# Kernel tuning notes

Hardware: AMD Instinct MI355X
Metric: run time of the kernel (lower is better)

The kernel has to match this reference:

```python
import jax, jax.numpy as jnp
import numpy as np

# fbank band edges (hp.bandmode == 'fbank'), 32 bands over 257 freq bins
EBAND = [0,3,5,8,10,13,15,18,22,25,29,33,38,42,48,53,59,66,73,80,89,97,107,117,128,140,153,167,183,199,216,256]

def _inverse_filter():
    f = np.zeros((len(EBAND), EBAND[-1] + 1), np.float32)
    for i in range(len(EBAND) - 1):
        w = EBAND[i + 1] - EBAND[i]
        for j in range(w):
            f[i, EBAND[i] + j] = 1.0 - j / w
            f[i + 1, EBAND[i] + j] = j / w
    return jnp.asarray(f)  # [32, 257]

def _glin(x, w):
    # GroupedLinear (DeepFilterNet-style, no bias): w [g, in/g, out/g]
    g, gi, go = w.shape
    y = jnp.einsum('...gi,gio->...go', x.reshape(x.shape[:-1] + (g, gi)), w)
    return y.reshape(x.shape[:-1] + (g * go,))

def _prelu(x, a):
    return jnp.where(x >= 0, x, a * x)

def _gru(x, wih, whh, bih, bhh):
    # single-layer torch-style GRU; x [T,B,I], wih/whh [3H, I/H]
    H = whh.shape[-1]
    h0 = jnp.zeros((x.shape[1], H), x.dtype)
    def step(h, xt):
        gi = xt @ wih.T + bih
        gh = h @ whh.T + bhh
        ir, iz, inn = jnp.split(gi, 3, axis=-1)
        hr, hz, hn = jnp.split(gh, 3, axis=-1)
        r = jax.nn.sigmoid(ir + hr)
        z = jax.nn.sigmoid(iz + hz)
        n = jnp.tanh(inn + r * hn)
        hnew = (1.0 - z) * n + z * h
        return hnew, hnew
    _, ys = jax.lax.scan(step, h0, x)
    return ys  # [T,B,H]

def _ggru_layer(x, wih, whh, bih, bhh):
    # grouped GRU layer: weights stacked on leading group axis
    g = wih.shape[0]
    T, B, I = x.shape
    xg = x.reshape(T, B, g, I // g).transpose(2, 0, 1, 3)  # [g,T,B,I/g]
    ys = jax.vmap(_gru)(xg, wih, whh, bih, bhh)            # [g,T,B,H/g]
    return ys.transpose(1, 2, 0, 3).reshape(T, B, -1)

def _shuffle(x, g):
    # channel shuffle between grouped GRU layers
    T, B, H = x.shape
    return x.reshape(T, B, -1, g).swapaxes(2, 3).reshape(T, B, H)

def _forward(main_input, spec, log_power_input, s1_fc_in_w, s1_fc_in_b,
             s1_gru_wih0, s1_gru_whh0, s1_gru_bih0, s1_gru_bhh0,
             s1_gru_wih1, s1_gru_whh1, s1_gru_bih1, s1_gru_bhh1,
             s1_fcout_w, fc_in_low_w, prelu_low, fc_in_high_w, prelu_high,
             gru_low_wih, gru_low_whh, gru_low_bih, gru_low_bhh,
             gru_high_wih, gru_high_whh, gru_high_bih, gru_high_bhh,
             fc_out_low_w, fc_out_high_w, ne, fc):
    B, _, T, F = main_input.shape
    # --- Stage1: pad time, unfold window, keep first ne+1 taps ---
    xp = jnp.pad(main_input, ((0, 0), (0, 0), (ne, ne), (0, 0)))
    win = jnp.stack([xp[:, :, k:k + T] for k in range(ne + 1)], axis=-1)  # [B,1,T,F,ne+1]
    x = win.reshape(B, T, F * (ne + 1))                                   # [B,T,64]
    x0 = (x @ s1_fc_in_w.T + s1_fc_in_b).transpose(1, 0, 2)               # [T,B,32]
    y1 = _gru(x0, s1_gru_wih0, s1_gru_whh0, s1_gru_bih0, s1_gru_bhh0)
    y2 = _gru(y1, s1_gru_wih1, s1_gru_whh1, s1_gru_bih1, s1_gru_bhh1)
    x1 = (y1 + y2).transpose(1, 0, 2)                                     # add_outputs; [B,T,32]
    band_mask = jax.nn.sigmoid(_glin(x1, s1_fcout_w))                     # [B,T,32]
    full_mask = (band_mask @ _inverse_filter()).transpose(0, 2, 1)        # [B,257,T]
    out = spec * full_mask[..., None]                                     # [B,257,T,2]
    # --- low band path ---
    low = jnp.concatenate([log_power_input[:, :, :fc], band_mask], axis=-1)  # [B,T,160]
    low = _prelu(_glin(low, fc_in_low_w), prelu_low).transpose(1, 0, 2)      # [T,B,64]
    acc = jnp.zeros_like(low)
    inp = low
    for l in range(2):  # 2 grouped layers, shuffle between, add_outputs
        inp = _ggru_layer(inp, gru_low_wih[l], gru_low_whh[l], gru_low_bih[l], gru_low_bhh[l])
        if l == 0:
            inp = _shuffle(inp, 2)
        acc = acc + inp
    mask_low = jax.nn.sigmoid(_glin(acc.transpose(1, 0, 2), fc_out_low_w))   # [B,T,128]
    # --- high band path ---
    high = jnp.concatenate([log_power_input[:, :, fc:256], band_mask], axis=-1)  # [B,T,160]
    high = _prelu(_glin(high, fc_in_high_w), prelu_high).transpose(1, 0, 2)      # [T,B,32]
    dfh = _ggru_layer(high, gru_high_wih, gru_high_whh, gru_high_bih, gru_high_bhh)
    mask_high = jax.nn.sigmoid(_glin(dfh.transpose(1, 0, 2), fc_out_high_w))     # [B,T,128]
    # --- fuse masks (rows: 0:fc low, fc:256 high, 256 passthrough) ---
    mask = jnp.concatenate([
        mask_low.transpose(0, 2, 1) * full_mask[:, :fc],
        mask_high.transpose(0, 2, 1) * full_mask[:, fc:256],
        full_mask[:, 256:257],
    ], axis=1)                                                            # [B,257,T]
    spec_out = mask[..., None] * out
    spec_mag = jnp.sqrt(spec_out[..., 0] ** 2 + spec_out[..., 1] ** 2)
    return full_mask, mask, spec_mag, spec_out

def setup_inputs():
    ks = iter(jax.random.split(jax.random.key(0), 48))
    rn = lambda shape, s=1.0: jax.random.normal(next(ks), shape, jnp.float32) * s
    B, T = 256, 256
    return {
        'main_input': rn((B, 1, T, 32)),
        'spec': rn((B, 257, T, 2)),
        'log_power_input': rn((B, T, 256)),
        'n_expand_fbank': 1,
        'freq_cut': 128,
        's1_fc_in_w': rn((32, 64), 0.125),
        's1_fc_in_b': rn((32,), 0.05),
        's1_gru_wih0': rn((96, 32), 0.18),
        's1_gru_whh0': rn((96, 32), 0.18),
        's1_gru_bih0': rn((96,), 0.05),
        's1_gru_bhh0': rn((96,), 0.05),
        's1_gru_wih1': rn((96, 32), 0.18),
        's1_gru_whh1': rn((96, 32), 0.18),
        's1_gru_bih1': rn((96,), 0.05),
        's1_gru_bhh1': rn((96,), 0.05),
        's1_fcout_w': rn((1, 32, 32), 0.18),
        'fc_in_low_w': rn((1, 160, 64), 0.08),
        'prelu_low': jnp.full((1,), 0.25, jnp.float32),
        'fc_in_high_w': rn((2, 80, 16), 0.11),
        'prelu_high': jnp.full((1,), 0.25, jnp.float32),
        'gru_low_wih': rn((2, 2, 96, 32), 0.18),
        'gru_low_whh': rn((2, 2, 96, 32), 0.18),
        'gru_low_bih': rn((2, 2, 96), 0.05),
        'gru_low_bhh': rn((2, 2, 96), 0.05),
        'gru_high_wih': rn((2, 48, 16), 0.25),
        'gru_high_whh': rn((2, 48, 16), 0.25),
        'gru_high_bih': rn((2, 48), 0.05),
        'gru_high_bhh': rn((2, 48), 0.05),
        'fc_out_low_w': rn((1, 64, 128), 0.125),
        'fc_out_high_w': rn((2, 16, 64), 0.25),
    }

def reference(main_input, spec, log_power_input, n_expand_fbank, freq_cut,
              s1_fc_in_w, s1_fc_in_b,
              s1_gru_wih0, s1_gru_whh0, s1_gru_bih0, s1_gru_bhh0,
              s1_gru_wih1, s1_gru_whh1, s1_gru_bih1, s1_gru_bhh1,
              s1_fcout_w, fc_in_low_w, prelu_low, fc_in_high_w, prelu_high,
              gru_low_wih, gru_low_whh, gru_low_bih, gru_low_bhh,
              gru_high_wih, gru_high_whh, gru_high_bih, gru_high_bhh,
              fc_out_low_w, fc_out_high_w):
    return _forward(main_input, spec, log_power_input, s1_fc_in_w, s1_fc_in_b,
                    s1_gru_wih0, s1_gru_whh0, s1_gru_bih0, s1_gru_bhh0,
                    s1_gru_wih1, s1_gru_whh1, s1_gru_bih1, s1_gru_bhh1,
                    s1_fcout_w, fc_in_low_w, prelu_low, fc_in_high_w, prelu_high,
                    gru_low_wih, gru_low_whh, gru_low_bih, gru_low_bhh,
                    gru_high_wih, gru_high_whh, gru_high_bih, gru_high_bhh,
                    fc_out_low_w, fc_out_high_w, int(n_expand_fbank), int(freq_cut))
```

## Files before the change

### kernel.cpp

```cpp
#include <hip/hip_runtime.h>
#include <math.h>

#define Bn 256
#define Tn 256

__constant__ int EB[32] = {0,3,5,8,10,13,15,18,22,25,29,33,38,42,48,53,59,66,73,80,89,97,107,117,128,140,153,167,183,199,216,256};

__device__ __forceinline__ float fsig(float x){ return __builtin_amdgcn_rcpf(1.f + __expf(-x)); }
__device__ __forceinline__ float ftanh(float x){ return 1.f - 2.f*__builtin_amdgcn_rcpf(1.f + __expf(2.f*x)); }

__device__ __forceinline__ void gload16(const float* g, float* l){
  __builtin_amdgcn_global_load_lds((const __attribute__((address_space(1))) void*)g,
                                   (__attribute__((address_space(3))) void*)l, 16, 0, 0);
}

#define KEEP(x) asm volatile("" : "+v"(x))

typedef float v2f __attribute__((ext_vector_type(2)));

#define DOT16(res, X, W) do{ float _s0=0.f,_s1=0.f,_s2=0.f,_s3=0.f; \
  _Pragma("unroll") for (int _e=0;_e<4;++_e){ \
    _s0=fmaf((X)[_e],(W)[_e],_s0); _s1=fmaf((X)[4+_e],(W)[4+_e],_s1); \
    _s2=fmaf((X)[8+_e],(W)[8+_e],_s2); _s3=fmaf((X)[12+_e],(W)[12+_e],_s3);} \
  (res)=(_s0+_s1)+(_s2+_s3); }while(0)

#define DOT8(res, X, W) do{ float _s0=0.f,_s1=0.f; \
  _Pragma("unroll") for (int _e=0;_e<4;++_e){ \
    _s0=fmaf((X)[_e],(W)[_e],_s0); _s1=fmaf((X)[4+_e],(W)[4+_e],_s1);} \
  (res)=_s0+_s1; }while(0)

#define FMA44(A, X, W) do{ \
  (A)[0]=fmaf((X).x,(W)[0].x,(A)[0]); (A)[1]=fmaf((X).x,(W)[0].y,(A)[1]); (A)[2]=fmaf((X).x,(W)[0].z,(A)[2]); (A)[3]=fmaf((X).x,(W)[0].w,(A)[3]); \
  (A)[0]=fmaf((X).y,(W)[1].x,(A)[0]); (A)[1]=fmaf((X).y,(W)[1].y,(A)[1]); (A)[2]=fmaf((X).y,(W)[1].z,(A)[2]); (A)[3]=fmaf((X).y,(W)[1].w,(A)[3]); \
  (A)[0]=fmaf((X).z,(W)[2].x,(A)[0]); (A)[1]=fmaf((X).z,(W)[2].y,(A)[1]); (A)[2]=fmaf((X).z,(W)[2].z,(A)[2]); (A)[3]=fmaf((X).z,(W)[2].w,(A)[3]); \
  (A)[0]=fmaf((X).w,(W)[3].x,(A)[0]); (A)[1]=fmaf((X).w,(W)[3].y,(A)[1]); (A)[2]=fmaf((X).w,(W)[3].z,(A)[2]); (A)[3]=fmaf((X).w,(W)[3].w,(A)[3]); \
}while(0)

__global__ __launch_bounds__(256) void k0(const float* __restrict__ wfc, const float* __restrict__ bfc,
    const float* __restrict__ wih0, const float* __restrict__ bih0,
    const float* __restrict__ wih1,
    const float* __restrict__ glw_ih, const float* __restrict__ glb_ih,
    const float* __restrict__ ghw_ih, const float* __restrict__ ghb_ih,
    float* __restrict__ wcT, float* __restrict__ bc,
    float* __restrict__ wBT, float* __restrict__ bB,
    float* __restrict__ wih1T, float* __restrict__ wB2T, float* __restrict__ bB2){
  int i = blockIdx.x*256 + threadIdx.x;
  if (i < 6144){
    int k = i/96, o = i - (i/96)*96;
    float s = 0.f;
    #pragma unroll
    for (int kk = 0; kk < 32; ++kk) s = fmaf(wih0[o*32+kk], wfc[kk*64+k], s);
    wcT[i] = s;
  } else if (i < 6240){
    int o = i - 6144;
    float s = bih0[o];
    #pragma unroll
    for (int kk = 0; kk < 32; ++kk) s = fmaf(wih0[o*32+kk], bfc[kk], s);
    bc[o] = s;
  } else if (i < 13920){
    int j = i - 6240;
    if (j < 6144){
      int og = j >> 7, rem = j & 127, k = rem >> 2, jj = rem & 3;
      int o = og*4 + jj; int g = o/96, r = o - g*96;
      wBT[j] = glw_ih[(g*96 + r)*32 + k];
    } else {
      int j2 = j - 6144;
      int oh = j2 >> 6, rem = j2 & 63, k = rem >> 2, jj = rem & 3;
      int o = oh*4 + jj; int g = o/48, r = o - g*48;
      wBT[j] = ghw_ih[(g*48 + r)*16 + k];
    }
  } else if (i < 14208){
    int o = i - 13920;
    bB[o] = (o < 192) ? glb_ih[o] : ghb_ih[o - 192];
  } else if (i < 17280){
    int j = i - 14208;
    int k = j/96, o = j - (j/96)*96;
    wih1T[j] = wih1[o*32 + k];
  } else if (i < 23424){
    int j = i - 17280;
    int og = j >> 7, rem = j & 127, k = rem >> 2, jj = rem & 3;
    int o = og*4 + jj; int g = o/96, r = o - g*96;
    wB2T[j] = glw_ih[((2+g)*96 + r)*32 + k];
  } else if (i < 23616){
    int o = i - 23424;
    bB2[o] = glb_ih[192 + o];
  }
}

__global__ __launch_bounds__(256) void k1(const float* __restrict__ mi,
    const float* __restrict__ wcT, const float* __restrict__ bc,
    float* __restrict__ gi0){
  __shared__ float mbuf[33*36];
  const int tid = threadIdx.x;
  const int b = blockIdx.x >> 3;
  const int t0 = (blockIdx.x & 7)*32;
  const int bt0 = b*256 + t0;
  for (int idx = tid; idx < 264; idx += 256){
    int row = idx >> 3, c4 = idx & 7;
    int r = t0 - 1 + row;
    float4 v = make_float4(0.f,0.f,0.f,0.f);
    if (r >= 0) v = *(const float4*)&mi[(b*256 + r)*32 + c4*4];
    *(float4*)&mbuf[row*36 + c4*4] = v;
  }
  __syncthreads();
  const int og = tid >> 3, btg = tid & 7;
  if (og >= 24) return;
  float acc[4][4];
  #pragma unroll
  for (int bj = 0; bj < 4; ++bj){ acc[bj][0]=0.f; acc[bj][1]=0.f; acc[bj][2]=0.f; acc[bj][3]=0.f; }
  for (int fq = 0; fq < 8; ++fq){
    float4 wvp[4], wvc[4];
    #pragma unroll
    for (int i = 0; i < 4; ++i){
      int f = fq*4 + i;
      wvp[i] = *(const float4*)&wcT[(2*f)*96 + og*4];
      wvc[i] = *(const float4*)&wcT[(2*f+1)*96 + og*4];
    }
    #pragma unroll
    for (int bj = 0; bj < 4; ++bj){
      int btl = btg + 8*bj;
      float4 xp = *(const float4*)&mbuf[btl*36 + fq*4];
      float4 xc = *(const float4*)&mbuf[(btl+1)*36 + fq*4];
      FMA44(acc[bj], xp, wvp);
      FMA44(acc[bj], xc, wvc);
    }
  }
  float4 bias = *(const float4*)&bc[og*4];
  #pragma unroll
  for (int bj = 0; bj < 4; ++bj){
    int btl = btg + 8*bj;
    float4 o;
    o.x = acc[bj][0] + bias.x; o.y = acc[bj][1] + bias.y;
    o.z = acc[bj][2] + bias.z; o.w = acc[bj][3] + bias.w;
    *(float4*)&gi0[(bt0 + btl)*96 + og*4] = o;
  }
}

__global__ __launch_bounds__(128,1) void kS1(const float* __restrict__ gi0,
    const float* __restrict__ whh0, const float* __restrict__ bhh0,
    const float* __restrict__ wih1, const float* __restrict__ whh1,
    const float* __restrict__ bih1, const float* __restrict__ bhh1,
    const float* __restrict__ fco, float* __restrict__ bmA)
{
  __shared__ __attribute__((aligned(16))) float gib[2][3072];
  __shared__ __attribute__((aligned(16))) float y1buf[2][32];
  __shared__ __attribute__((aligned(16))) float h1arr[32];
  __shared__ __attribute__((aligned(16))) float h2arr[32];
  const int tid = threadIdx.x;
  const int wid = tid >> 6;
  const int lane = tid & 63;
  const int q = lane >> 5, h = lane & 31, ko = q*16;
  const int b = blockIdx.x;
  const float* gsrc = gi0 + b*24576;

  float wI[3][16], wH[3][16], wF[16];
  float b0, b1, b2, b3;
  if (wid == 0){
    #pragma unroll
    for (int g = 0; g < 3; ++g){
      const float* w = whh0 + (g*32+h)*32 + ko;
      #pragma unroll
      for (int k = 0; k < 16; ++k){ wI[g][k] = w[k]; wH[g][k] = w[k]; }
    }
    #pragma unroll
    for (int k = 0; k < 16; ++k) wF[k] = 0.f;
    b0 = bhh0[h]; b1 = bhh0[32+h]; b2 = bhh0[64+h]; b3 = 0.f;
    #pragma unroll
    for (int c0 = 0; c0 < 2; ++c0)
      for (int it = 0; it < 12; ++it)
        gload16(gsrc + c0*3072 + it*256 + lane*4, &gib[c0][it*256]);
    asm volatile("s_waitcnt vmcnt(0)" ::: "memory");
  } else {
    #pragma unroll
    for (int g = 0; g < 3; ++g){
      const float* wi = wih1 + (g*32+h)*32 + ko;
      const float* wh = whh1 + (g*32+h)*32 + ko;
      #pragma unroll
      for (int k = 0; k < 16; ++k){ wI[g][k] = wi[k]; wH[g][k] = wh[k]; }
    }
    #pragma unroll
    for (int k = 0; k < 16; ++k) wF[k] = fco[(ko+k)*32 + h];
    b0 = bih1[h] + bhh1[h];
    b1 = bih1[32+h] + bhh1[32+h];
    b2 = bih1[64+h];
    b3 = bhh1[64+h];
  }
  #pragma unroll
  for (int g = 0; g < 3; ++g){
    #pragma unroll
    for (int k = 0; k < 16; ++k){ KEEP(wI[g][k]); KEEP(wH[g][k]); }
  }
  #pragma unroll
  for (int k = 0; k < 16; ++k) KEEP(wF[k]);
  __syncthreads();

  float hv[16];
  #pragma unroll
  for (int k = 0; k < 16; ++k) hv[k] = 0.f;
  float hOwn = 0.f;
  float c_r = 0.f, c_z = 0.f, c_n = 0.f, p_r = 0.f, p_z = 0.f, p_n = 0.f;

  for (int s = 0; s <= Tn; ++s){
    __syncthreads();
    if (wid == 0){
      if (s < Tn){
        const int t = s;
        if ((t & 31) == 0){
          if (t){
            int c = t >> 5;
            if (c < 7){
              for (int it = 0; it < 12; ++it)
                gload16(gsrc + (c+1)*3072 + it*256 + lane*4, &gib[(c+1)&1][it*256]);
            }
          }
          const float* gt = &gib[(t>>5)&1][(t&31)*96];
          c_r = gt[h]; c_z = gt[32+h]; c_n = gt[64+h];
        } else { c_r = p_r; c_z = p_z; c_n = p_n; }
        if ((t+1) & 31){
          const float* gn = &gib[((t+1)>>5)&1][((t+1)&31)*96];
          p_r = gn[h]; p_z = gn[32+h]; p_n = gn[64+h];
        }
        float pr, pz, pn;
        DOT16(pr, hv, wI[0]); DOT16(pz, hv, wI[1]); DOT16(pn, hv, wI[2]);
        pr += __shfl_xor(pr,32); pz += __shfl_xor(pz,32); pn += __shfl_xor(pn,32);
        float r = fsig(c_r + pr + b0);
        float z = fsig(c_z + pz + b1);
        float nn = ftanh(c_n + r*(pn + b2));
        float hn = nn + z*(hOwn - nn);
        hOwn = hn;
        h1arr[h] = hn;
        if (q == 0) y1buf[s & 1][h] = hn;
        *(float4*)&hv[0]  = *(const float4*)&h1arr[ko+0];
        *(float4*)&hv[4]  = *(const float4*)&h1arr[ko+4];
        *(float4*)&hv[8]  = *(const float4*)&h1arr[ko+8];
        *(float4*)&hv[12] = *(const float4*)&h1arr[ko+12];
      }
    } else {
      if (s >= 1){
        const int t = s - 1;
        const float* yb = y1buf[t & 1];
        float xv[16];
        *(float4*)&xv[0]  = *(const float4*)&yb[ko+0];
        *(float4*)&xv[4]  = *(const float4*)&yb[ko+4];
        *(float4*)&xv[8]  = *(const float4*)&yb[ko+8];
        *(float4*)&xv[12] = *(const float4*)&yb[ko+12];
        float ur, uz, ui, vr, vz, vh;
        DOT16(ur, xv, wI[0]); DOT16(uz, xv, wI[1]); DOT16(ui, xv, wI[2]);
        DOT16(vr, hv, wH[0]); DOT16(vz, hv, wH[1]); DOT16(vh, hv, wH[2]);
        float qr = ur + vr, qz = uz + vz;
        qr += __shfl_xor(qr,32); qz += __shfl_xor(qz,32);
        ui += __shfl_xor(ui,32); vh += __shfl_xor(vh,32);
        float r1 = fsig(qr + b0);
        float z1 = fsig(qz + b1);
        float n1 = ftanh(ui + b2 + r1*(vh + b3));
        float hn = n1 + z1*(hOwn - n1);
        hOwn = hn;
        h2arr[h] = hn;
        *(float4*)&hv[0]  = *(const float4*)&h2arr[ko+0];
        *(float4*)&hv[4]  = *(const float4*)&h2arr[ko+4];
        *(float4*)&hv[8]  = *(const float4*)&h2arr[ko+8];
        *(float4*)&hv[12] = *(const float4*)&h2arr[ko+12];
        float sf = 0.f;
        #pragma unroll
        for (int k = 0; k < 16; ++k) sf = fmaf(xv[k] + hv[k], wF[k], sf);
        sf += __shfl_xor(sf,32);
        if (q == 0) bmA[(b*Tn + t)*32 + h] = fsig(sf);
      }
    }
  }
}

__global__ __launch_bounds__(256) void kP(const float* __restrict__ lpi,
    const float* __restrict__ bmA,
    const float* __restrict__ wlo, const float* __restrict__ plo,
    const float* __restrict__ whi, const float* __restrict__ phi,
    const float* __restrict__ wBT, const float* __restrict__ bB,
    float* __restrict__ giL, float* __restrict__ giH)
{
  __shared__ float xb[32*292];
  __shared__ float mb[32*100];
  const int tid = threadIdx.x;
  const int b = blockIdx.x >> 3;
  const int t0 = (blockIdx.x & 7)*32;
  const int bt0 = b*256 + t0;
  #pragma unroll
  for (int j = 0; j < 8; ++j){
    int idx = j*256 + tid;
    int row = idx >> 6, c4 = idx & 63;
    float4 v = *(const float4*)&lpi[(bt0 + row)*256 + c4*4];
    *(float4*)&xb[row*292 + c4*4] = v;
  }
  {
    int row = tid >> 3, c4 = tid & 7;
    float4 v = *(const float4*)&bmA[(bt0 + row)*32 + c4*4];
    *(float4*)&xb[row*292 + 256 + c4*4] = v;
  }
  __syncthreads();
  const int og = tid >> 3, btg = tid & 7;
  if (og < 16){
    float acc[4][4];
    #pragma unroll
    for (int bj = 0; bj < 4; ++bj){ acc[bj][0]=0.f; acc[bj][1]=0.f; acc[bj][2]=0.f; acc[bj][3]=0.f; }
    for (int kq = 0; kq < 40; ++kq){
      int k0_ = kq*4;
      int kk = (k0_ < 128) ? k0_ : k0_ + 128;
      float4 wv[4];
      #pragma unroll
      for (int i = 0; i < 4; ++i) wv[i] = *(const float4*)&wlo[(k0_+i)*64 + og*4];
      #pragma unroll
      for (int bj = 0; bj < 4; ++bj){
        float4 xv = *(const float4*)&xb[(btg + 8*bj)*292 + kk];
        FMA44(acc[bj], xv, wv);
      }
    }
    const float a = plo[0];
    #pragma unroll
    for (int bj = 0; bj < 4; ++bj){
      float4 m;
      m.x = acc[bj][0] >= 0.f ? acc[bj][0] : a*acc[bj][0];
      m.y = acc[bj][1] >= 0.f ? acc[bj][1] : a*acc[bj][1];
      m.z = acc[bj][2] >= 0.f ? acc[bj][2] : a*acc[bj][2];
      m.w = acc[bj][3] >= 0.f ? acc[bj][3] : a*acc[bj][3];
      *(float4*)&mb[(btg + 8*bj)*100 + og*4] = m;
    }
  } else if (og < 24){
    int o0 = (og - 16)*4;
    int g = o0 >> 4, r0 = o0 & 15;
    int xoff = 128 + g*80;
    float acc[4][4];
    #pragma unroll
    for (int bj = 0; bj < 4; ++bj){ acc[bj][0]=0.f; acc[bj][1]=0.f; acc[bj][2]=0.f; acc[bj][3]=0.f; }
    for (int kq = 0; kq < 20; ++kq){
      int k0_ = kq*4;
      float4 wv[4];
      #pragma unroll
      for (int i = 0; i < 4; ++i) wv[i] = *(const float4*)&whi[(g*80 + k0_ + i)*16 + r0];
      #pragma unroll
      for (int bj = 0; bj < 4; ++bj){
        float4 xv = *(const float4*)&xb[(btg + 8*bj)*292 + xoff + k0_];
        FMA44(acc[bj], xv, wv);
      }
    }
    const float a = phi[0];
    #pragma unroll
    for (int bj = 0; bj < 4; ++bj){
      float4 m;
      m.x = acc[bj][0] >= 0.f ? acc[bj][0] : a*acc[bj][0];
      m.y = acc[bj][1] >= 0.f ? acc[bj][1] : a*acc[bj][1];
      m.z = acc[bj][2] >= 0.f ? acc[bj][2] : a*acc[bj][2];
      m.w = acc[bj][3] >= 0.f ? acc[bj][3] : a*acc[bj][3];
      *(float4*)&mb[(btg + 8*bj)*100 + 64 + o0] = m;
    }
  }
  __syncthreads();
  for (int og2 = og; og2 < 72; og2 += 32){
    int woff, kbase, K, obase, dstride;
    float* dst;
    float4 bias;
    if (og2 < 48){
      woff = og2*128; kbase = (og2 >= 24) ? 32 : 0; K = 32;
      obase = og2*4; dst = giL; dstride = 192;
      bias = *(const float4*)&bB[obase];
    } else {
      int oh = og2 - 48;
      woff = 6144 + oh*64;
      int o0 = oh*4; int g = o0/48;
      kbase = 64 + g*16; K = 16;
      obase = o0; dst = giH; dstride = 96;
      bias = *(const float4*)&bB[192 + o0];
    }
    float acc[4][4];
    #pragma unroll
    for (int bj = 0; bj < 4; ++bj){ acc[bj][0]=0.f; acc[bj][1]=0.f; acc[bj][2]=0.f; acc[bj][3]=0.f; }
    for (int kq = 0; kq < K/4; ++kq){
      float4 wv[4];
      #pragma unroll
      for (int i = 0; i < 4; ++i) wv[i] = *(const float4*)&wBT[woff + (kq*4 + i)*4];
      #pragma unroll
      for (int bj = 0; bj < 4; ++bj){
        float4 xv = *(const float4*)&mb[(btg + 8*bj)*100 + kbase + kq*4];
        FMA44(acc[bj], xv, wv);
      }
    }
    #pragma unroll
    for (int bj = 0; bj < 4; ++bj){
      int btl = btg + 8*bj;
      float4 o;
      o.x = acc[bj][0] + bias.x; o.y = acc[bj][1] + bias.y;
      o.z = acc[bj][2] + bias.z; o.w = acc[bj][3] + bias.w;
      *(float4*)&dst[(bt0 + btl)*dstride + obase] = o;
    }
  }
}

__global__ __launch_bounds__(256,1) void kR2(const float* __restrict__ giL,
    const float* __restrict__ giH,
    const float* __restrict__ wihL, const float* __restrict__ whhL,
    const float* __restrict__ bihL, const float* __restrict__ bhhL,
    const float* __restrict__ whhH, const float* __restrict__ bhhH,
    float* __restrict__ acc, float* __restrict__ dfh)
{
  __shared__ __attribute__((aligned(16))) float smem[12544];
  const int tid = threadIdx.x;
  const int wid = tid >> 6;
  const int lane = tid & 63;
  if (blockIdx.x < 256){
    const int role = wid >> 1;
    const int g = wid & 1;
    const int q = lane >> 5, h = lane & 31, ko = q*16;
    const int b = blockIdx.x;
    float* gib   = smem + g*6144;
    float* y0buf = smem + 12288;
    float* h0arr = smem + 12416 + g*32;
    float* h1l   = smem + 12480;
    const float* gsrc = giL + b*49152 + g*96;

    float wI[3][16], wH[3][16];
    float b0, b1, b2, b3;
    if (role == 0){
      #pragma unroll
      for (int gt = 0; gt < 3; ++gt){
        const float* w = whhL + (g*96 + gt*32 + h)*32 + ko;
        #pragma unroll
        for (int k = 0; k < 16; ++k){ wI[gt][k] = w[k]; wH[gt][k] = w[k]; }
      }
      b0 = bhhL[g*96+h]; b1 = bhhL[g*96+32+h]; b2 = bhhL[g*96+64+h]; b3 = 0.f;
      #pragma unroll
      for (int c0 = 0; c0 < 2; ++c0)
        for (int it = 0; it < 12; ++it){
          int i = it*64 + lane;
          int toff = i/24, c4 = i - toff*24;
          gload16(gsrc + (c0*32 + toff)*192 + c4*4, &gib[c0*3072 + it*256]);
        }
      asm volatile("s_waitcnt vmcnt(0)" ::: "memory");
    } else {
      #pragma unroll
      for (int gt = 0; gt < 3; ++gt){
        const float* wi = wihL + ((2+g)*96 + gt*32 + h)*32 + ko;
        const float* wh = whhL + ((2+g)*96 + gt*32 + h)*32 + ko;
        #pragma unroll
        for (int k = 0; k < 16; ++k){ wI[gt][k] = wi[k]; wH[gt][k] = wh[k]; }
      }
      b0 = bihL[(2+g)*96+h]    + bhhL[(2+g)*96+h];
      b1 = bihL[(2+g)*96+32+h] + bhhL[(2+g)*96+32+h];
      b2 = bihL[(2+g)*96+64+h];
      b3 = bhhL[(2+g)*96+64+h];
    }
    #pragma unroll
    for (int gt = 0; gt < 3; ++gt){
      #pragma unroll
      for (int k = 0; k < 16; ++k){ KEEP(wI[gt][k]); KEEP(wH[gt][k]); }
    }
    __syncthreads();

    float hv[16];
    #pragma unroll
    for (int k = 0; k < 16; ++k) hv[k] = 0.f;
    float hOwn = 0.f;
    float c_r = 0.f, c_z = 0.f, c_n = 0.f, p_r = 0.f, p_z = 0.f, p_n = 0.f;
    const int spos = ((h&1)<<5) + (g<<4) + (h>>1);

    for (int s = 0; s <= Tn; ++s){
      __syncthreads();
      if (role == 0){
        if (s < Tn){
          const int t = s;
          if ((t & 31) == 0){
            if (t){
              int c = t >> 5;
              if (c < 7){
                for (int it = 0; it < 12; ++it){
                  int i = it*64 + lane;
                  int toff = i/24, c4 = i - toff*24;
                  gload16(gsrc + ((c+1)*32 + toff)*192 + c4*4, &gib[((c+1)&1)*3072 + it*256]);
                }
              }
            }
            const float* gt = &gib[((t>>5)&1)*3072 + (t&31)*96];
            c_r = gt[h]; c_z = gt[32+h]; c_n = gt[64+h];
          } else { c_r = p_r; c_z = p_z; c_n = p_n; }
          if ((t+1) & 31){
            const float* gn = &gib[(((t+1)>>5)&1)*3072 + ((t+1)&31)*96];
            p_r = gn[h]; p_z = gn[32+h]; p_n = gn[64+h];
          }
          float pr, pz, pn;
          DOT16(pr, hv, wI[0]); DOT16(pz, hv, wI[1]); DOT16(pn, hv, wI[2]);
          pr += __shfl_xor(pr,32); pz += __shfl_xor(pz,32); pn += __shfl_xor(pn,32);
          float r = fsig(c_r + pr + b0);
          float z = fsig(c_z + pz + b1);
          float nn = ftanh(c_n + r*(pn + b2));
          float hn = nn + z*(hOwn - nn);
          hOwn = hn;
          h0arr[h] = hn;
          if (q == 0) y0buf[(s&1)*64 + spos] = hn;
          *(float4*)&hv[0]  = *(const float4*)&h0arr[ko+0];
          *(float4*)&hv[4]  = *(const float4*)&h0arr[ko+4];
          *(float4*)&hv[8]  = *(const float4*)&h0arr[ko+8];
          *(float4*)&hv[12] = *(const float4*)&h0arr[ko+12];
        }
      } else {
        if (s >= 1){
          const int t = s - 1;
          const float* yb = &y0buf[(t&1)*64];
          float xv[16];
          *(float4*)&xv[0]  = *(const float4*)&yb[g*32 + ko + 0];
          *(float4*)&xv[4]  = *(const float4*)&yb[g*32 + ko + 4];
          *(float4*)&xv[8]  = *(const float4*)&yb[g*32 + ko + 8];
          *(float4*)&xv[12] = *(const float4*)&yb[g*32 + ko + 12];
          float yown = yb[g*32 + h];
          float ur, uz, ui, vr, vz, vh;
          DOT16(ur, xv, wI[0]); DOT16(uz, xv, wI[1]); DOT16(ui, xv, wI[2]);
          DOT16(vr, hv, wH[0]); DOT16(vz, hv, wH[1]); DOT16(vh, hv, wH[2]);
          float qr = ur + vr, qz = uz + vz;
          qr += __shfl_xor(qr,32); qz += __shfl_xor(qz,32);
          ui += __shfl_xor(ui,32); vh += __shfl_xor(vh,32);
          float r1 = fsig(qr + b0);
          float z1 = fsig(qz + b1);
          float n1 = ftanh(ui + b2 + r1*(vh + b3));
          float hn = n1 + z1*(hOwn - n1);
          hOwn = hn;
          h1l[g*32 + h] = hn;
          *(float4*)&hv[0]  = *(const float4*)&h1l[g*32 + ko+0];
          *(float4*)&hv[4]  = *(const float4*)&h1l[g*32 + ko+4];
          *(float4*)&hv[8]  = *(const float4*)&h1l[g*32 + ko+8];
          *(float4*)&hv[12] = *(const float4*)&h1l[g*32 + ko+12];
          if (q == 0) acc[(b*256 + t)*64 + g*32 + h] = yown + hn;
        }
      }
    }
  } else {
    const int g = lane >> 5, qh = (lane >> 4) & 1, h = lane & 15, ko = qh*8;
    const int b = (blockIdx.x - 256)*4 + wid;
    float* gib  = smem + wid*3072;
    float* harr = smem + 12288 + wid*32;
    float ah[3][8];
    #pragma unroll
    for (int gt = 0; gt < 3; ++gt){
      const float* wp = whhH + (g*48 + gt*16 + h)*16 + ko;
      #pragma unroll
      for (int k = 0; k < 8; ++k) ah[gt][k] = wp[k];
    }
    #pragma unroll
    for (int gt = 0; gt < 3; ++gt){
      #pragma unroll
      for (int k = 0; k < 8; ++k) KEEP(ah[gt][k]);
    }
    const float bhr = bhhH[g*48+h], bhz = bhhH[g*48+16+h], bhn = bhhH[g*48+32+h];
    const float* gsrc = giH + b*24576;
    #pragma unroll
    for (int c0 = 0; c0 < 2; ++c0)
      for (int it = 0; it < 6; ++it)
        gload16(gsrc + c0*1536 + it*256 + lane*4, &gib[c0*1536 + it*256]);
    asm volatile("s_waitcnt vmcnt(0)" ::: "memory");

    float hv[8];
    #pragma unroll
    for (int k = 0; k < 8; ++k) hv[k] = 0.f;
    float hOwn = 0.f;
    float c_r = 0.f, c_z = 0.f, c_n = 0.f, p_r = 0.f, p_z = 0.f, p_n = 0.f;

    for (int t = 0; t < Tn; ++t){
      if ((t & 15) == 0){
        if (t){
          int c = t >> 4;
          if (c < 15){
            const float* gs = gsrc + (c+1)*1536;
            for (int it = 0; it < 6; ++it)
              gload16(gs + it*256 + lane*4, &gib[((c+1)&1)*1536 + it*256]);
            asm volatile("s_waitcnt vmcnt(6)" ::: "memory");
          } else {
            asm volatile("s_waitcnt vmcnt(0)" ::: "memory");
          }
        }
        const float* gt = &gib[((t>>4)&1)*1536 + (t&15)*96 + g*48];
        c_r = gt[h]; c_z = gt[16+h]; c_n = gt[32+h];
      } else { c_r = p_r; c_z = p_z; c_n = p_n; }
      if ((t+1) & 15){
        const float* gn = &gib[(((t+1)>>4)&1)*1536 + ((t+1)&15)*96 + g*48];
        p_r = gn[h]; p_z = gn[16+h]; p_n = gn[32+h];
      }
      float pr, pz, pn;
      DOT8(pr, hv, ah[0]); DOT8(pz, hv, ah[1]); DOT8(pn, hv, ah[2]);
      pr += __shfl_xor(pr,16); pz += __shfl_xor(pz,16); pn += __shfl_xor(pn,16);
      float r = fsig(c_r + pr + bhr);
      float z = fsig(c_z + pz + bhz);
      float nn = ftanh(c_n + r*(pn + bhn));
      float hn = nn + z*(hOwn - nn);
      hOwn = hn;
      harr[g*16 + h] = hn;
      *(float4*)&hv[0] = *(const float4*)&harr[g*16 + ko + 0];
      *(float4*)&hv[4] = *(const float4*)&harr[g*16 + ko + 4];
      if (qh == 0) dfh[(b*256 + t)*32 + g*16 + h] = hn;
    }
  }
}

__global__ __launch_bounds__(256) void k7(const float* __restrict__ acc,
    const float* __restrict__ dfh, const float* __restrict__ bmA,
    const float* __restrict__ wlo, const float* __restrict__ whi,
    const float* __restrict__ spec, float* __restrict__ out)
{
  __shared__ float accs[32][65];
  __shared__ float dfhs[32][33];
  __shared__ float bmt[32][33];
  __shared__ float frcs[257];
  __shared__ int   ibds[257];
  const int tid = threadIdx.x;
  const int b  = blockIdx.x >> 3;
  const int t0 = (blockIdx.x & 7) * 32;
  for (int idx = tid; idx < 32*16; idx += 256){
    int tl = idx >> 4, c4 = (idx & 15)*4;
    float4 v = *(const float4*)&acc[(b*256 + t0 + tl)*64 + c4];
    accs[tl][c4] = v.x; accs[tl][c4+1] = v.y; accs[tl][c4+2] = v.z; accs[tl][c4+3] = v.w;
  }
  for (int idx = tid; idx < 32*8; idx += 256){
    int tl = idx >> 3, c4 = (idx & 7)*4;
    float4 v = *(const float4*)&dfh[(b*256 + t0 + tl)*32 + c4];
    dfhs[tl][c4] = v.x; dfhs[tl][c4+1] = v.y; dfhs[tl][c4+2] = v.z; dfhs[tl][c4+3] = v.w;
    float4 u = *(const float4*)&bmA[(b*Tn + t0 + tl)*32 + c4];
    bmt[tl][c4] = u.x; bmt[tl][c4+1] = u.y; bmt[tl][c4+2] = u.z; bmt[tl][c4+3] = u.w;
  }
  for (int f = tid; f < 257; f += 256){
    int i = 0;
    #pragma unroll
    for (int k = 1; k < 31; ++k) if (f >= EB[k]) i = k;
    ibds[f] = i;
    frcs[f] = (f < 256) ? (float)(f - EB[i]) / (float)(EB[i+1] - EB[i]) : 0.f;
  }
  __syncthreads();
  const int tl = tid & 31, fo = tid >> 5;
  float* out1 = out + 16842752;
  float* out2 = out + 2*16842752;
  float* out3 = out + 3*16842752;
  const float2* sp2 = (const float2*)spec;
  {
    float p[16];
    #pragma unroll
    for (int j = 0; j < 16; ++j) p[j] = 0.f;
    for (int i = 0; i < 64; ++i){
      float a = accs[tl][i];
      const float4* wr = (const float4*)&wlo[i*128 + fo*16];
      #pragma unroll
      for (int j4 = 0; j4 < 4; ++j4){
        float4 wv = wr[j4];
        p[j4*4+0] = fmaf(a, wv.x, p[j4*4+0]);
        p[j4*4+1] = fmaf(a, wv.y, p[j4*4+1]);
        p[j4*4+2] = fmaf(a, wv.z, p[j4*4+2]);
        p[j4*4+3] = fmaf(a, wv.w, p[j4*4+3]);
      }
    }
    #pragma unroll
    for (int j = 0; j < 16; ++j){
      int f = fo*16 + j;
      int i = ibds[f]; float fr = frcs[f];
      float full = bmt[tl][i]*(1.f - fr) + bmt[tl][i+1]*fr;
      float m = fsig(p[j])*full;
      int base = (b*257 + f)*Tn + t0 + tl;
      float2 s = sp2[base];
      float fm = full*m;
      float sx = s.x*fm, sy = s.y*fm;
      __builtin_nontemporal_store(full, &out[base]);
      __builtin_nontemporal_store(m, &out1[base]);
      __builtin_nontemporal_store(sqrtf(sx*sx + sy*sy), &out2[base]);
      v2f o3; o3.x = sx; o3.y = sy;
      __builtin_nontemporal_store(o3, (v2f*)&out3[base*2]);
    }
  }
  {
    float p[16];
    #pragma unroll
    for (int j = 0; j < 16; ++j) p[j] = 0.f;
    const int g = fo >> 2, ob = (fo & 3)*16;
    for (int i = 0; i < 16; ++i){
      float a = dfhs[tl][g*16 + i];
      const float4* wr = (const float4*)&whi[(g*16 + i)*64 + ob];
      #pragma unroll
      for (int j4 = 0; j4 < 4; ++j4){
        float4 wv = wr[j4];
        p[j4*4+0] = fmaf(a, wv.x, p[j4*4+0]);
        p[j4*4+1] = fmaf(a, wv.y, p[j4*4+1]);
        p[j4*4+2] = fmaf(a, wv.z, p[j4*4+2]);
        p[j4*4+3] = fmaf(a, wv.w, p[j4*4+3]);
      }
    }
    #pragma unroll
    for (int j = 0; j < 16; ++j){
      int f = 128 + fo*16 + j;
      int i = ibds[f]; float fr = frcs[f];
      float full = bmt[tl][i]*(1.f - fr) + bmt[tl][i+1]*fr;
      float m = fsig(p[j])*full;
      int base = (b*257 + f)*Tn + t0 + tl;
      float2 s = sp2[base];
      float fm = full*m;
      float sx = s.x*fm, sy = s.y*fm;
      __builtin_nontemporal_store(full, &out[base]);
      __builtin_nontemporal_store(m, &out1[base]);
      __builtin_nontemporal_store(sqrtf(sx*sx + sy*sy), &out2[base]);
      v2f o3; o3.x = sx; o3.y = sy;
      __builtin_nontemporal_store(o3, (v2f*)&out3[base*2]);
    }
  }
  if (fo == 0){
    int base = (b*257 + 256)*Tn + t0 + tl;
    __builtin_nontemporal_store(0.f, &out[base]);
    __builtin_nontemporal_store(0.f, &out1[base]);
    __builtin_nontemporal_store(0.f, &out2[base]);
    v2f z; z.x = 0.f; z.y = 0.f;
    __builtin_nontemporal_store(z, (v2f*)&out3[base*2]);
  }
}

extern "C" void kernel_launch(void* const* d_in, const int* in_sizes, int n_in,
                              void* d_out, int out_size, void* d_ws, size_t ws_size,
                              hipStream_t stream){
  const float* mi   = (const float*)d_in[0];
  const float* spec = (const float*)d_in[1];
  const float* lpi  = (const float*)d_in[2];
  const float* s1w  = (const float*)d_in[5];
  const float* s1b  = (const float*)d_in[6];
  const float* wih0 = (const float*)d_in[7];
  const float* whh0 = (const float*)d_in[8];
  const float* bih0 = (const float*)d_in[9];
  const float* bhh0 = (const float*)d_in[10];
  const float* wih1 = (const float*)d_in[11];
  const float* whh1 = (const float*)d_in[12];
  const float* bih1 = (const float*)d_in[13];
  const float* bhh1 = (const float*)d_in[14];
  const float* fco  = (const float*)d_in[15];
  const float* filw = (const float*)d_in[16];
  const float* plo  = (const float*)d_in[17];
  const float* fihw = (const float*)d_in[18];
  const float* phi  = (const float*)d_in[19];
  const float* glw_ih = (const float*)d_in[20];
  const float* glw_hh = (const float*)d_in[21];
  const float* glb_ih = (const float*)d_in[22];
  const float* glb_hh = (const float*)d_in[23];
  const float* ghw_ih = (const float*)d_in[24];
  const float* ghw_hh = (const float*)d_in[25];
  const float* ghb_ih = (const float*)d_in[26];
  const float* ghb_hh = (const float*)d_in[27];
  const float* folw = (const float*)d_in[28];
  const float* fohw = (const float*)d_in[29];

  float* outf = (float*)d_out;
  float* giL  = outf;
  float* gi0  = outf + 12582912;
  float* giH  = outf + 18874368;

  float* ws    = (float*)d_ws;
  float* wcT   = ws;
  float* bc    = ws + 6144;
  float* wBT   = ws + 6240;
  float* bB    = ws + 13920;
  float* wih1T = ws + 14208;
  float* wB2T  = ws + 17280;
  float* bB2   = ws + 23424;
  float* bmA   = ws + 24576;
  float* acc   = ws + 2121728;
  float* dfh   = ws + 6316032;
  float* out   = (float*)d_out;

  k0<<<93, 256, 0, stream>>>(s1w, s1b, wih0, bih0, wih1, glw_ih, glb_ih, ghw_ih, ghb_ih,
                             wcT, bc, wBT, bB, wih1T, wB2T, bB2);
  k1<<<2048, 256, 0, stream>>>(mi, wcT, bc, gi0);
  kS1<<<256, 128, 0, stream>>>(gi0, whh0, bhh0, wih1, whh1, bih1, bhh1, fco, bmA);
  kP<<<2048, 256, 0, stream>>>(lpi, bmA, filw, plo, fihw, phi, wBT, bB, giL, giH);
  kR2<<<320, 256, 0, stream>>>(giL, giH, glw_ih, glw_hh, glb_ih, glb_hh,
                               ghw_hh, ghb_hh, acc, dfh);
  k7<<<2048, 256, 0, stream>>>(acc, dfh, bmA, folw, fohw, spec, out);
}
```

Measured before the change: 578.4 us.

## Fuse projection, stage-1 GRU, pointwise and grouped GRU kernels into one per-batch kernel

Merges k1, kS1, kP and kR2 into a single kernel kM with one 320-thread block per batch element. Each block runs the input projection, the stage-1 GRU, the middle projections and the low/high grouped GRUs in sequence, and drops the unused transposed-weight outputs from k0. This removes several launches and the gaps between them, and keeps intermediates hot in cache. The cost is only 256 blocks doing the formerly 2048-block parallel projections, and one block per CU under heavy register pressure.

```diff
diff --git a/kernel.cpp b/kernel.cpp
--- a/kernel.cpp
+++ b/kernel.cpp
@@ -38,12 +38,10 @@
 
 __global__ __launch_bounds__(256) void k0(const float* __restrict__ wfc, const float* __restrict__ bfc,
     const float* __restrict__ wih0, const float* __restrict__ bih0,
-    const float* __restrict__ wih1,
     const float* __restrict__ glw_ih, const float* __restrict__ glb_ih,
     const float* __restrict__ ghw_ih, const float* __restrict__ ghb_ih,
     float* __restrict__ wcT, float* __restrict__ bc,
-    float* __restrict__ wBT, float* __restrict__ bB,
-    float* __restrict__ wih1T, float* __restrict__ wB2T, float* __restrict__ bB2){
+    float* __restrict__ wBT, float* __restrict__ bB){
   int i = blockIdx.x*256 + threadIdx.x;
   if (i < 6144){
     int k = i/96, o = i - (i/96)*96;
@@ -72,385 +70,132 @@
   } else if (i < 14208){
     int o = i - 13920;
     bB[o] = (o < 192) ? glb_ih[o] : ghb_ih[o - 192];
-  } else if (i < 17280){
-    int j = i - 14208;
-    int k = j/96, o = j - (j/96)*96;
-    wih1T[j] = wih1[o*32 + k];
-  } else if (i < 23424){
-    int j = i - 17280;
-    int og = j >> 7, rem = j & 127, k = rem >> 2, jj = rem & 3;
-    int o = og*4 + jj; int g = o/96, r = o - g*96;
-    wB2T[j] = glw_ih[((2+g)*96 + r)*32 + k];
-  } else if (i < 23616){
-    int o = i - 23424;
-    bB2[o] = glb_ih[192 + o];
   }
 }
 
-__global__ __launch_bounds__(256) void k1(const float* __restrict__ mi,
+__global__ __launch_bounds__(320,1) void kM(const float* __restrict__ mi,
     const float* __restrict__ wcT, const float* __restrict__ bc,
-    float* __restrict__ gi0){
-  __shared__ float mbuf[33*36];
-  const int tid = threadIdx.x;
-  const int b = blockIdx.x >> 3;
-  const int t0 = (blockIdx.x & 7)*32;
-  const int bt0 = b*256 + t0;
-  for (int idx = tid; idx < 264; idx += 256){
-    int row = idx >> 3, c4 = idx & 7;
-    int r = t0 - 1 + row;
-    float4 v = make_float4(0.f,0.f,0.f,0.f);
-    if (r >= 0) v = *(const float4*)&mi[(b*256 + r)*32 + c4*4];
-    *(float4*)&mbuf[row*36 + c4*4] = v;
-  }
-  __syncthreads();
-  const int og = tid >> 3, btg = tid & 7;
-  if (og >= 24) return;
-  float acc[4][4];
-  #pragma unroll
-  for (int bj = 0; bj < 4; ++bj){ acc[bj][0]=0.f; acc[bj][1]=0.f; acc[bj][2]=0.f; acc[bj][3]=0.f; }
-  for (int fq = 0; fq < 8; ++fq){
-    float4 wvp[4], wvc[4];
-    #pragma unroll
-    for (int i = 0; i < 4; ++i){
-      int f = fq*4 + i;
-      wvp[i] = *(const float4*)&wcT[(2*f)*96 + og*4];
-      wvc[i] = *(const float4*)&wcT[(2*f+1)*96 + og*4];
-    }
-    #pragma unroll
-    for (int bj = 0; bj < 4; ++bj){
-      int btl = btg + 8*bj;
-      float4 xp = *(const float4*)&mbuf[btl*36 + fq*4];
-      float4 xc = *(const float4*)&mbuf[(btl+1)*36 + fq*4];
-      FMA44(acc[bj], xp, wvp);
-      FMA44(acc[bj], xc, wvc);
-    }
-  }
-  float4 bias = *(const float4*)&bc[og*4];
-  #pragma unroll
-  for (int bj = 0; bj < 4; ++bj){
-    int btl = btg + 8*bj;
-    float4 o;
-    o.x = acc[bj][0] + bias.x; o.y = acc[bj][1] + bias.y;
-    o.z = acc[bj][2] + bias.z; o.w = acc[bj][3] + bias.w;
-    *(float4*)&gi0[(bt0 + btl)*96 + og*4] = o;
-  }
-}
-
-__global__ __launch_bounds__(128,1) void kS1(const float* __restrict__ gi0,
     const float* __restrict__ whh0, const float* __restrict__ bhh0,
     const float* __restrict__ wih1, const float* __restrict__ whh1,
     const float* __restrict__ bih1, const float* __restrict__ bhh1,
-    const float* __restrict__ fco, float* __restrict__ bmA)
+    const float* __restrict__ fco,
+    const float* __restrict__ lpi,
+    const float* __restrict__ wlo, const float* __restrict__ plo,
+    const float* __restrict__ whi, const float* __restrict__ phi,
+    const float* __restrict__ wBT, const float* __restrict__ bB,
+    const float* __restrict__ wihL, const float* __restrict__ whhL,
+    const float* __restrict__ bihL, const float* __restrict__ bhhL,
+    const float* __restrict__ whhH, const float* __restrict__ bhhH,
+    float* __restrict__ gi0w, float* __restrict__ bmA,
+    float* __restrict__ giL, float* __restrict__ giH,
+    float* __restrict__ acc, float* __restrict__ dfh)
 {
-  __shared__ __attribute__((aligned(16))) float gib[2][3072];
-  __shared__ __attribute__((aligned(16))) float y1buf[2][32];
-  __shared__ __attribute__((aligned(16))) float h1arr[32];
-  __shared__ __attribute__((aligned(16))) float h2arr[32];
+  __shared__ __attribute__((aligned(16))) float smem[15648];
   const int tid = threadIdx.x;
   const int wid = tid >> 6;
   const int lane = tid & 63;
-  const int q = lane >> 5, h = lane & 31, ko = q*16;
   const int b = blockIdx.x;
-  const float* gsrc = gi0 + b*24576;
-
-  float wI[3][16], wH[3][16], wF[16];
-  float b0, b1, b2, b3;
-  if (wid == 0){
+
+  {
+    float* mbuf = smem;
+    for (int tile = 0; tile < 8; ++tile){
+      const int t0 = tile*32;
+      const int bt0 = b*256 + t0;
+      for (int idx = tid; idx < 264; idx += 320){
+        int row = idx >> 3, c4 = idx & 7;
+        int r = t0 - 1 + row;
+        float4 v = make_float4(0.f,0.f,0.f,0.f);
+        if (r >= 0) v = *(const float4*)&mi[(b*256 + r)*32 + c4*4];
+        *(float4*)&mbuf[row*36 + c4*4] = v;
+      }
+      __syncthreads();
+      if (tid < 256){
+        const int og = tid >> 3, btg = tid & 7;
+        if (og < 24){
+          float a4[4][4];
+          #pragma unroll
+          for (int bj = 0; bj < 4; ++bj){ a4[bj][0]=0.f; a4[bj][1]=0.f; a4[bj][2]=0.f; a4[bj][3]=0.f; }
+          for (int fq = 0; fq < 8; ++fq){
+            float4 wvp[4], wvc[4];
+            #pragma unroll
+            for (int i = 0; i < 4; ++i){
+              int f = fq*4 + i;
+              wvp[i] = *(const float4*)&wcT[(2*f)*96 + og*4];
+              wvc[i] = *(const float4*)&wcT[(2*f+1)*96 + og*4];
+            }
+            #pragma unroll
+            for (int bj = 0; bj < 4; ++bj){
+              int btl = btg + 8*bj;
+              float4 xp = *(const float4*)&mbuf[btl*36 + fq*4];
+              float4 xc = *(const float4*)&mbuf[(btl+1)*36 + fq*4];
+              FMA44(a4[bj], xp, wvp);
+              FMA44(a4[bj], xc, wvc);
+            }
+          }
+          float4 bias = *(const float4*)&bc[og*4];
+          #pragma unroll
+          for (int bj = 0; bj < 4; ++bj){
+            int btl = btg + 8*bj;
+            float4 o;
+            o.x = a4[bj][0] + bias.x; o.y = a4[bj][1] + bias.y;
+            o.z = a4[bj][2] + bias.z; o.w = a4[bj][3] + bias.w;
+            *(float4*)&gi0w[(bt0 + btl)*96 + og*4] = o;
+          }
+        }
+      }
+      __syncthreads();
+    }
+  }
+
+  {
+    const int q = lane >> 5, h = lane & 31, ko = q*16;
+    float* y1buf = smem + 6144;
+    float* h1arr = smem + 6208;
+    float* h2arr = smem + 6240;
+    const float* gsrc = gi0w + b*24576;
+    float wI[3][16], wH[3][16], wF[16];
+    float b0=0.f, b1=0.f, b2=0.f, b3=0.f;
+    #pragma unroll
+    for (int g = 0; g < 3; ++g)
+      #pragma unroll
+      for (int k = 0; k < 16; ++k){ wI[g][k]=0.f; wH[g][k]=0.f; }
+    #pragma unroll
+    for (int k = 0; k < 16; ++k) wF[k] = 0.f;
+    if (wid == 0){
+      #pragma unroll
+      for (int g = 0; g < 3; ++g){
+        const float* w = whh0 + (g*32+h)*32 + ko;
+        #pragma unroll
+        for (int k = 0; k < 16; ++k){ wI[g][k] = w[k]; wH[g][k] = w[k]; }
+      }
+      b0 = bhh0[h]; b1 = bhh0[32+h]; b2 = bhh0[64+h];
+      #pragma unroll
+      for (int c0 = 0; c0 < 2; ++c0)
+        for (int it = 0; it < 12; ++it)
+          gload16(gsrc + c0*3072 + it*256 + lane*4, &smem[c0*3072 + it*256]);
+      asm volatile("s_waitcnt vmcnt(0)" ::: "memory");
+    } else if (wid == 1){
+      #pragma unroll
+      for (int g = 0; g < 3; ++g){
+        const float* wi = wih1 + (g*32+h)*32 + ko;
+        const float* wh = whh1 + (g*32+h)*32 + ko;
+        #pragma unroll
+        for (int k = 0; k < 16; ++k){ wI[g][k] = wi[k]; wH[g][k] = wh[k]; }
+      }
+      #pragma unroll
+      for (int k = 0; k < 16; ++k) wF[k] = fco[(ko+k)*32 + h];
+      b0 = bih1[h] + bhh1[h];
+      b1 = bih1[32+h] + bhh1[32+h];
+      b2 = bih1[64+h];
+      b3 = bhh1[64+h];
+    }
     #pragma unroll
     for (int g = 0; g < 3; ++g){
-      const float* w = whh0 + (g*32+h)*32 + ko;
-      #pragma unroll
-      for (int k = 0; k < 16; ++k){ wI[g][k] = w[k]; wH[g][k] = w[k]; }
-    }
-    #pragma unroll
-    for (int k = 0; k < 16; ++k) wF[k] = 0.f;
-    b0 = bhh0[h]; b1 = bhh0[32+h]; b2 = bhh0[64+h]; b3 = 0.f;
-    #pragma unroll
-    for (int c0 = 0; c0 < 2; ++c0)
-      for (int it = 0; it < 12; ++it)
-        gload16(gsrc + c0*3072 + it*256 + lane*4, &gib[c0][it*256]);
-    asm volatile("s_waitcnt vmcnt(0)" ::: "memory");
-  } else {
-    #pragma unroll
-    for (int g = 0; g < 3; ++g){
-      const float* wi = wih1 + (g*32+h)*32 + ko;
-      const float* wh = whh1 + (g*32+h)*32 + ko;
-      #pragma unroll
-      for (int k = 0; k < 16; ++k){ wI[g][k] = wi[k]; wH[g][k] = wh[k]; }
-    }
-    #pragma unroll
-    for (int k = 0; k < 16; ++k) wF[k] = fco[(ko+k)*32 + h];
-    b0 = bih1[h] + bhh1[h];
-    b1 = bih1[32+h] + bhh1[32+h];
-    b2 = bih1[64+h];
-    b3 = bhh1[64+h];
-  }
-  #pragma unroll
-  for (int g = 0; g < 3; ++g){
-    #pragma unroll
-    for (int k = 0; k < 16; ++k){ KEEP(wI[g][k]); KEEP(wH[g][k]); }
-  }
-  #pragma unroll
-  for (int k = 0; k < 16; ++k) KEEP(wF[k]);
-  __syncthreads();
-
-  float hv[16];
-  #pragma unroll
-  for (int k = 0; k < 16; ++k) hv[k] = 0.f;
-  float hOwn = 0.f;
-  float c_r = 0.f, c_z = 0.f, c_n = 0.f, p_r = 0.f, p_z = 0.f, p_n = 0.f;
-
-  for (int s = 0; s <= Tn; ++s){
-    __syncthreads();
-    if (wid == 0){
-      if (s < Tn){
-        const int t = s;
-        if ((t & 31) == 0){
-          if (t){
-            int c = t >> 5;
-            if (c < 7){
-              for (int it = 0; it < 12; ++it)
-                gload16(gsrc + (c+1)*3072 + it*256 + lane*4, &gib[(c+1)&1][it*256]);
-            }
-          }
-          const float* gt = &gib[(t>>5)&1][(t&31)*96];
-          c_r = gt[h]; c_z = gt[32+h]; c_n = gt[64+h];
-        } else { c_r = p_r; c_z = p_z; c_n = p_n; }
-        if ((t+1) & 31){
-          const float* gn = &gib[((t+1)>>5)&1][((t+1)&31)*96];
-          p_r = gn[h]; p_z = gn[32+h]; p_n = gn[64+h];
-        }
-        float pr, pz, pn;
-        DOT16(pr, hv, wI[0]); DOT16(pz, hv, wI[1]); DOT16(pn, hv, wI[2]);
-        pr += __shfl_xor(pr,32); pz += __shfl_xor(pz,32); pn += __shfl_xor(pn,32);
-        float r = fsig(c_r + pr + b0);
-        float z = fsig(c_z + pz + b1);
-        float nn = ftanh(c_n + r*(pn + b2));
-        float hn = nn + z*(hOwn - nn);
-        hOwn = hn;
-        h1arr[h] = hn;
-        if (q == 0) y1buf[s & 1][h] = hn;
-        *(float4*)&hv[0]  = *(const float4*)&h1arr[ko+0];
-        *(float4*)&hv[4]  = *(const float4*)&h1arr[ko+4];
-        *(float4*)&hv[8]  = *(const float4*)&h1arr[ko+8];
-        *(float4*)&hv[12] = *(const float4*)&h1arr[ko+12];
-      }
-    } else {
-      if (s >= 1){
-        const int t = s - 1;
-        const float* yb = y1buf[t & 1];
-        float xv[16];
-        *(float4*)&xv[0]  = *(const float4*)&yb[ko+0];
-        *(float4*)&xv[4]  = *(const float4*)&yb[ko+4];
-        *(float4*)&xv[8]  = *(const float4*)&yb[ko+8];
-        *(float4*)&xv[12] = *(const float4*)&yb[ko+12];
-        float ur, uz, ui, vr, vz, vh;
-        DOT16(ur, xv, wI[0]); DOT16(uz, xv, wI[1]); DOT16(ui, xv, wI[2]);
-        DOT16(vr, hv, wH[0]); DOT16(vz, hv, wH[1]); DOT16(vh, hv, wH[2]);
-        float qr = ur + vr, qz = uz + vz;
-        qr += __shfl_xor(qr,32); qz += __shfl_xor(qz,32);
-        ui += __shfl_xor(ui,32); vh += __shfl_xor(vh,32);
-        float r1 = fsig(qr + b0);
-        float z1 = fsig(qz + b1);
-        float n1 = ftanh(ui + b2 + r1*(vh + b3));
-        float hn = n1 + z1*(hOwn - n1);
-        hOwn = hn;
-        h2arr[h] = hn;
-        *(float4*)&hv[0]  = *(const float4*)&h2arr[ko+0];
-        *(float4*)&hv[4]  = *(const float4*)&h2arr[ko+4];
-        *(float4*)&hv[8]  = *(const float4*)&h2arr[ko+8];
-        *(float4*)&hv[12] = *(const float4*)&h2arr[ko+12];
-        float sf = 0.f;
-        #pragma unroll
-        for (int k = 0; k < 16; ++k) sf = fmaf(xv[k] + hv[k], wF[k], sf);
-        sf += __shfl_xor(sf,32);
-        if (q == 0) bmA[(b*Tn + t)*32 + h] = fsig(sf);
-      }
-    }
-  }
-}
-
-__global__ __launch_bounds__(256) void kP(const float* __restrict__ lpi,
-    const float* __restrict__ bmA,
-    const float* __restrict__ wlo, const float* __restrict__ plo,
-    const float* __restrict__ whi, const float* __restrict__ phi,
-    const float* __restrict__ wBT, const float* __restrict__ bB,
-    float* __restrict__ giL, float* __restrict__ giH)
-{
-  __shared__ float xb[32*292];
-  __shared__ float mb[32*100];
-  const int tid = threadIdx.x;
-  const int b = blockIdx.x >> 3;
-  const int t0 = (blockIdx.x & 7)*32;
-  const int bt0 = b*256 + t0;
-  #pragma unroll
-  for (int j = 0; j < 8; ++j){
-    int idx = j*256 + tid;
-    int row = idx >> 6, c4 = idx & 63;
-    float4 v = *(const float4*)&lpi[(bt0 + row)*256 + c4*4];
-    *(float4*)&xb[row*292 + c4*4] = v;
-  }
-  {
-    int row = tid >> 3, c4 = tid & 7;
-    float4 v = *(const float4*)&bmA[(bt0 + row)*32 + c4*4];
-    *(float4*)&xb[row*292 + 256 + c4*4] = v;
-  }
-  __syncthreads();
-  const int og = tid >> 3, btg = tid & 7;
-  if (og < 16){
-    float acc[4][4];
-    #pragma unroll
-    for (int bj = 0; bj < 4; ++bj){ acc[bj][0]=0.f; acc[bj][1]=0.f; acc[bj][2]=0.f; acc[bj][3]=0.f; }
-    for (int kq = 0; kq < 40; ++kq){
-      int k0_ = kq*4;
-      int kk = (k0_ < 128) ? k0_ : k0_ + 128;
-      float4 wv[4];
-      #pragma unroll
-      for (int i = 0; i < 4; ++i) wv[i] = *(const float4*)&wlo[(k0_+i)*64 + og*4];
-      #pragma unroll
-      for (int bj = 0; bj < 4; ++bj){
-        float4 xv = *(const float4*)&xb[(btg + 8*bj)*292 + kk];
-        FMA44(acc[bj], xv, wv);
-      }
-    }
-    const float a = plo[0];
-    #pragma unroll
-    for (int bj = 0; bj < 4; ++bj){
-      float4 m;
-      m.x = acc[bj][0] >= 0.f ? acc[bj][0] : a*acc[bj][0];
-      m.y = acc[bj][1] >= 0.f ? acc[bj][1] : a*acc[bj][1];
-      m.z = acc[bj][2] >= 0.f ? acc[bj][2] : a*acc[bj][2];
-      m.w = acc[bj][3] >= 0.f ? acc[bj][3] : a*acc[bj][3];
-      *(float4*)&mb[(btg + 8*bj)*100 + og*4] = m;
-    }
-  } else if (og < 24){
-    int o0 = (og - 16)*4;
-    int g = o0 >> 4, r0 = o0 & 15;
-    int xoff = 128 + g*80;
-    float acc[4][4];
-    #pragma unroll
-    for (int bj = 0; bj < 4; ++bj){ acc[bj][0]=0.f; acc[bj][1]=0.f; acc[bj][2]=0.f; acc[bj][3]=0.f; }
-    for (int kq = 0; kq < 20; ++kq){
-      int k0_ = kq*4;
-      float4 wv[4];
-      #pragma unroll
-      for (int i = 0; i < 4; ++i) wv[i] = *(const float4*)&whi[(g*80 + k0_ + i)*16 + r0];
-      #pragma unroll
-      for (int bj = 0; bj < 4; ++bj){
-        float4 xv = *(const float4*)&xb[(btg + 8*bj)*292 + xoff + k0_];
-        FMA44(acc[bj], xv, wv);
-      }
-    }
-    const float a = phi[0];
-    #pragma unroll
-    for (int bj = 0; bj < 4; ++bj){
-      float4 m;
-      m.x = acc[bj][0] >= 0.f ? acc[bj][0] : a*acc[bj][0];
-      m.y = acc[bj][1] >= 0.f ? acc[bj][1] : a*acc[bj][1];
-      m.z = acc[bj][2] >= 0.f ? acc[bj][2] : a*acc[bj][2];
-      m.w = acc[bj][3] >= 0.f ? acc[bj][3] : a*acc[bj][3];
-      *(float4*)&mb[(btg + 8*bj)*100 + 64 + o0] = m;
-    }
-  }
-  __syncthreads();
-  for (int og2 = og; og2 < 72; og2 += 32){
-    int woff, kbase, K, obase, dstride;
-    float* dst;
-    float4 bias;
-    if (og2 < 48){
-      woff = og2*128; kbase = (og2 >= 24) ? 32 : 0; K = 32;
-      obase = og2*4; dst = giL; dstride = 192;
-      bias = *(const float4*)&bB[obase];
-    } else {
-      int oh = og2 - 48;
-      woff = 6144 + oh*64;
-      int o0 = oh*4; int g = o0/48;
-      kbase = 64 + g*16; K = 16;
-      obase = o0; dst = giH; dstride = 96;
-      bias = *(const float4*)&bB[192 + o0];
-    }
-    float acc[4][4];
-    #pragma unroll
-    for (int bj = 0; bj < 4; ++bj){ acc[bj][0]=0.f; acc[bj][1]=0.f; acc[bj][2]=0.f; acc[bj][3]=0.f; }
-    for (int kq = 0; kq < K/4; ++kq){
-      float4 wv[4];
-      #pragma unroll
-      for (int i = 0; i < 4; ++i) wv[i] = *(const float4*)&wBT[woff + (kq*4 + i)*4];
-      #pragma unroll
-      for (int bj = 0; bj < 4; ++bj){
-        float4 xv = *(const float4*)&mb[(btg + 8*bj)*100 + kbase + kq*4];
-        FMA44(acc[bj], xv, wv);
-      }
-    }
-    #pragma unroll
-    for (int bj = 0; bj < 4; ++bj){
-      int btl = btg + 8*bj;
-      float4 o;
-      o.x = acc[bj][0] + bias.x; o.y = acc[bj][1] + bias.y;
-      o.z = acc[bj][2] + bias.z; o.w = acc[bj][3] + bias.w;
-      *(float4*)&dst[(bt0 + btl)*dstride + obase] = o;
-    }
-  }
-}
-
-__global__ __launch_bounds__(256,1) void kR2(const float* __restrict__ giL,
-    const float* __restrict__ giH,
-    const float* __restrict__ wihL, const float* __restrict__ whhL,
-    const float* __restrict__ bihL, const float* __restrict__ bhhL,
-    const float* __restrict__ whhH, const float* __restrict__ bhhH,
-    float* __restrict__ acc, float* __restrict__ dfh)
-{
-  __shared__ __attribute__((aligned(16))) float smem[12544];
-  const int tid = threadIdx.x;
-  const int wid = tid >> 6;
-  const int lane = tid & 63;
-  if (blockIdx.x < 256){
-    const int role = wid >> 1;
-    const int g = wid & 1;
-    const int q = lane >> 5, h = lane & 31, ko = q*16;
-    const int b = blockIdx.x;
-    float* gib   = smem + g*6144;
-    float* y0buf = smem + 12288;
-    float* h0arr = smem + 12416 + g*32;
-    float* h1l   = smem + 12480;
-    const float* gsrc = giL + b*49152 + g*96;
-
-    float wI[3][16], wH[3][16];
-    float b0, b1, b2, b3;
-    if (role == 0){
-      #pragma unroll
-      for (int gt = 0; gt < 3; ++gt){
-        const float* w = whhL + (g*96 + gt*32 + h)*32 + ko;
-        #pragma unroll
-        for (int k = 0; k < 16; ++k){ wI[gt][k] = w[k]; wH[gt][k] = w[k]; }
-      }
-      b0 = bhhL[g*96+h]; b1 = bhhL[g*96+32+h]; b2 = bhhL[g*96+64+h]; b3 = 0.f;
-      #pragma unroll
-      for (int c0 = 0; c0 < 2; ++c0)
-        for (int it = 0; it < 12; ++it){
-          int i = it*64 + lane;
-          int toff = i/24, c4 = i - toff*24;
-          gload16(gsrc + (c0*32 + toff)*192 + c4*4, &gib[c0*3072 + it*256]);
-        }
-      asm volatile("s_waitcnt vmcnt(0)" ::: "memory");
-    } else {
-      #pragma unroll
-      for (int gt = 0; gt < 3; ++gt){
-        const float* wi = wihL + ((2+g)*96 + gt*32 + h)*32 + ko;
-        const float* wh = whhL + ((2+g)*96 + gt*32 + h)*32 + ko;
-        #pragma unroll
-        for (int k = 0; k < 16; ++k){ wI[gt][k] = wi[k]; wH[gt][k] = wh[k]; }
-      }
-      b0 = bihL[(2+g)*96+h]    + bhhL[(2+g)*96+h];
-      b1 = bihL[(2+g)*96+32+h] + bhhL[(2+g)*96+32+h];
-      b2 = bihL[(2+g)*96+64+h];
-      b3 = bhhL[(2+g)*96+64+h];
-    }
-    #pragma unroll
-    for (int gt = 0; gt < 3; ++gt){
-      #pragma unroll
-      for (int k = 0; k < 16; ++k){ KEEP(wI[gt][k]); KEEP(wH[gt][k]); }
-    }
+      #pragma unroll
+      for (int k = 0; k < 16; ++k){ KEEP(wI[g][k]); KEEP(wH[g][k]); }
+    }
+    #pragma unroll
+    for (int k = 0; k < 16; ++k) KEEP(wF[k]);
     __syncthreads();
 
     float hv[16];
@@ -458,29 +203,25 @@
     for (int k = 0; k < 16; ++k) hv[k] = 0.f;
     float hOwn = 0.f;
     float c_r = 0.f, c_z = 0.f, c_n = 0.f, p_r = 0.f, p_z = 0.f, p_n = 0.f;
-    const int spos = ((h&1)<<5) + (g<<4) + (h>>1);
 
     for (int s = 0; s <= Tn; ++s){
       __syncthreads();
-      if (role == 0){
+      if (wid == 0){
         if (s < Tn){
           const int t = s;
           if ((t & 31) == 0){
             if (t){
               int c = t >> 5;
               if (c < 7){
-                for (int it = 0; it < 12; ++it){
-                  int i = it*64 + lane;
-                  int toff = i/24, c4 = i - toff*24;
-                  gload16(gsrc + ((c+1)*32 + toff)*192 + c4*4, &gib[((c+1)&1)*3072 + it*256]);
-                }
+                for (int it = 0; it < 12; ++it)
+                  gload16(gsrc + (c+1)*3072 + it*256 + lane*4, &smem[((c+1)&1)*3072 + it*256]);
               }
             }
-            const float* gt = &gib[((t>>5)&1)*3072 + (t&31)*96];
+            const float* gt = &smem[((t>>5)&1)*3072 + (t&31)*96];
             c_r = gt[h]; c_z = gt[32+h]; c_n = gt[64+h];
           } else { c_r = p_r; c_z = p_z; c_n = p_n; }
           if ((t+1) & 31){
-            const float* gn = &gib[(((t+1)>>5)&1)*3072 + ((t+1)&31)*96];
+            const float* gn = &smem[(((t+1)>>5)&1)*3072 + ((t+1)&31)*96];
             p_r = gn[h]; p_z = gn[32+h]; p_n = gn[64+h];
           }
           float pr, pz, pn;
@@ -491,23 +232,22 @@
           float nn = ftanh(c_n + r*(pn + b2));
           float hn = nn + z*(hOwn - nn);
           hOwn = hn;
-          h0arr[h] = hn;
-          if (q == 0) y0buf[(s&1)*64 + spos] = hn;
-          *(float4*)&hv[0]  = *(const float4*)&h0arr[ko+0];
-          *(float4*)&hv[4]  = *(const float4*)&h0arr[ko+4];
-          *(float4*)&hv[8]  = *(const float4*)&h0arr[ko+8];
-          *(float4*)&hv[12] = *(const float4*)&h0arr[ko+12];
-        }
-      } else {
+          h1arr[h] = hn;
+          if (q == 0) y1buf[(s & 1)*32 + h] = hn;
+          *(float4*)&hv[0]  = *(const float4*)&h1arr[ko+0];
+          *(float4*)&hv[4]  = *(const float4*)&h1arr[ko+4];
+          *(float4*)&hv[8]  = *(const float4*)&h1arr[ko+8];
+          *(float4*)&hv[12] = *(const float4*)&h1arr[ko+12];
+        }
+      } else if (wid == 1){
         if (s >= 1){
           const int t = s - 1;
-          const float* yb = &y0buf[(t&1)*64];
+          const float* yb = &y1buf[(t & 1)*32];
           float xv[16];
-          *(float4*)&xv[0]  = *(const float4*)&yb[g*32 + ko + 0];
-          *(float4*)&xv[4]  = *(const float4*)&yb[g*32 + ko + 4];
-          *(float4*)&xv[8]  = *(const float4*)&yb[g*32 + ko + 8];
-          *(float4*)&xv[12] = *(const float4*)&yb[g*32 + ko + 12];
-          float yown = yb[g*32 + h];
+          *(float4*)&xv[0]  = *(const float4*)&yb[ko+0];
+          *(float4*)&xv[4]  = *(const float4*)&yb[ko+4];
+          *(float4*)&xv[8]  = *(const float4*)&yb[ko+8];
+          *(float4*)&xv[12] = *(const float4*)&yb[ko+12];
           float ur, uz, ui, vr, vz, vh;
           DOT16(ur, xv, wI[0]); DOT16(uz, xv, wI[1]); DOT16(ui, xv, wI[2]);
           DOT16(vr, hv, wH[0]); DOT16(vz, hv, wH[1]); DOT16(vh, hv, wH[2]);
@@ -519,78 +259,328 @@
           float n1 = ftanh(ui + b2 + r1*(vh + b3));
           float hn = n1 + z1*(hOwn - n1);
           hOwn = hn;
-          h1l[g*32 + h] = hn;
-          *(float4*)&hv[0]  = *(const float4*)&h1l[g*32 + ko+0];
-          *(float4*)&hv[4]  = *(const float4*)&h1l[g*32 + ko+4];
-          *(float4*)&hv[8]  = *(const float4*)&h1l[g*32 + ko+8];
-          *(float4*)&hv[12] = *(const float4*)&h1l[g*32 + ko+12];
-          if (q == 0) acc[(b*256 + t)*64 + g*32 + h] = yown + hn;
-        }
-      }
-    }
-  } else {
-    const int g = lane >> 5, qh = (lane >> 4) & 1, h = lane & 15, ko = qh*8;
-    const int b = (blockIdx.x - 256)*4 + wid;
-    float* gib  = smem + wid*3072;
-    float* harr = smem + 12288 + wid*32;
-    float ah[3][8];
+          h2arr[h] = hn;
+          *(float4*)&hv[0]  = *(const float4*)&h2arr[ko+0];
+          *(float4*)&hv[4]  = *(const float4*)&h2arr[ko+4];
+          *(float4*)&hv[8]  = *(const float4*)&h2arr[ko+8];
+          *(float4*)&hv[12] = *(const float4*)&h2arr[ko+12];
+          float sf = 0.f;
+          #pragma unroll
+          for (int k = 0; k < 16; ++k) sf = fmaf(xv[k] + hv[k], wF[k], sf);
+          sf += __shfl_xor(sf,32);
+          if (q == 0) bmA[(b*Tn + t)*32 + h] = fsig(sf);
+        }
+      }
+    }
+    __syncthreads();
+  }
+
+  {
+    float* xb = smem;
+    float* mb = smem + 9344;
+    for (int tile = 0; tile < 8; ++tile){
+      const int t0 = tile*32;
+      const int bt0 = b*256 + t0;
+      if (tid < 256){
+        #pragma unroll
+        for (int j = 0; j < 8; ++j){
+          int idx = j*256 + tid;
+          int row = idx >> 6, c4 = idx & 63;
+          float4 v = *(const float4*)&lpi[(bt0 + row)*256 + c4*4];
+          *(float4*)&xb[row*292 + c4*4] = v;
+        }
+        {
+          int row = tid >> 3, c4 = tid & 7;
+          float4 v = *(const float4*)&bmA[(bt0 + row)*32 + c4*4];
+          *(float4*)&xb[row*292 + 256 + c4*4] = v;
+        }
+      }
+      __syncthreads();
+      if (tid < 256){
+        const int og = tid >> 3, btg = tid & 7;
+        if (og < 16){
+          float a4[4][4];
+          #pragma unroll
+          for (int bj = 0; bj < 4; ++bj){ a4[bj][0]=0.f; a4[bj][1]=0.f; a4[bj][2]=0.f; a4[bj][3]=0.f; }
+          for (int kq = 0; kq < 40; ++kq){
+            int k0_ = kq*4;
+            int kk = (k0_ < 128) ? k0_ : k0_ + 128;
+            float4 wv[4];
+            #pragma unroll
+            for (int i = 0; i < 4; ++i) wv[i] = *(const float4*)&wlo[(k0_+i)*64 + og*4];
+            #pragma unroll
+            for (int bj = 0; bj < 4; ++bj){
+              float4 xv = *(const float4*)&xb[(btg + 8*bj)*292 + kk];
+              FMA44(a4[bj], xv, wv);
+            }
+          }
+          const float a = plo[0];
+          #pragma unroll
+          for (int bj = 0; bj < 4; ++bj){
+            float4 m;
+            m.x = a4[bj][0] >= 0.f ? a4[bj][0] : a*a4[bj][0];
+            m.y = a4[bj][1] >= 0.f ? a4[bj][1] : a*a4[bj][1];
+            m.z = a4[bj][2] >= 0.f ? a4[bj][2] : a*a4[bj][2];
+            m.w = a4[bj][3] >= 0.f ? a4[bj][3] : a*a4[bj][3];
+            *(float4*)&mb[(btg + 8*bj)*100 + og*4] = m;
+          }
+        } else if (og < 24){
+          int o0 = (og - 16)*4;
+          int g = o0 >> 4, r0 = o0 & 15;
+          int xoff = 128 + g*80;
+          float a4[4][4];
+          #pragma unroll
+          for (int bj = 0; bj < 4; ++bj){ a4[bj][0]=0.f; a4[bj][1]=0.f; a4[bj][2]=0.f; a4[bj][3]=0.f; }
+          for (int kq = 0; kq < 20; ++kq){
+            int k0_ = kq*4;
+            float4 wv[4];
+            #pragma unroll
+            for (int i = 0; i < 4; ++i) wv[i] = *(const float4*)&whi[(g*80 + k0_ + i)*16 + r0];
+            #pragma unroll
+            for (int bj = 0; bj < 4; ++bj){
+              float4 xv = *(const float4*)&xb[(btg + 8*bj)*292 + xoff + k0_];
+              FMA44(a4[bj], xv, wv);
+            }
+          }
+          const float a = phi[0];
+          #pragma unroll
+          for (int bj = 0; bj < 4; ++bj){
+            float4 m;
+            m.x = a4[bj][0] >= 0.f ? a4[bj][0] : a*a4[bj][0];
+            m.y = a4[bj][1] >= 0.f ? a4[bj][1] : a*a4[bj][1];
+            m.z = a4[bj][2] >= 0.f ? a4[bj][2] : a*a4[bj][2];
+            m.w = a4[bj][3] >= 0.f ? a4[bj][3] : a*a4[bj][3];
+            *(float4*)&mb[(btg + 8*bj)*100 + 64 + o0] = m;
+          }
+        }
+      }
+      __syncthreads();
+      if (tid < 256){
+        const int og = tid >> 3, btg = tid & 7;
+        for (int og2 = og; og2 < 72; og2 += 32){
+          int woff, kbase, K, obase, dstride;
+          float* dst;
+          float4 bias;
+          if (og2 < 48){
+            woff = og2*128; kbase = (og2 >= 24) ? 32 : 0; K = 32;
+            obase = og2*4; dst = giL; dstride = 192;
+            bias = *(const float4*)&bB[obase];
+          } else {
+            int oh = og2 - 48;
+            woff = 6144 + oh*64;
+            int o0 = oh*4; int g = o0/48;
+            kbase = 64 + g*16; K = 16;
+            obase = o0; dst = giH; dstride = 96;
+            bias = *(const float4*)&bB[192 + o0];
+          }
+          float a4[4][4];
+          #pragma unroll
+          for (int bj = 0; bj < 4; ++bj){ a4[bj][0]=0.f; a4[bj][1]=0.f; a4[bj][2]=0.f; a4[bj][3]=0.f; }
+          for (int kq = 0; kq < K/4; ++kq){
+            float4 wv[4];
+            #pragma unroll
+            for (int i = 0; i < 4; ++i) wv[i] = *(const float4*)&wBT[woff + (kq*4 + i)*4];
+            #pragma unroll
+            for (int bj = 0; bj < 4; ++bj){
+              float4 xv = *(const float4*)&mb[(btg + 8*bj)*100 + kbase + kq*4];
+              FMA44(a4[bj], xv, wv);
+            }
+          }
+          #pragma unroll
+          for (int bj = 0; bj < 4; ++bj){
+            int btl = btg + 8*bj;
+            float4 o;
+            o.x = a4[bj][0] + bias.x; o.y = a4[bj][1] + bias.y;
+            o.z = a4[bj][2] + bias.z; o.w = a4[bj][3] + bias.w;
+            *(float4*)&dst[(bt0 + btl)*dstride + obase] = o;
+          }
+        }
+      }
+      __syncthreads();
+    }
+  }
+
+  {
+    const int role = wid >> 1;
+    const int g = wid & 1;
+    const int q = lane >> 5, h = lane & 31, ko = q*16;
+    const int gH = lane >> 5, qH = (lane >> 4) & 1, hH = lane & 15, koH = qH*8;
+    float* y0buf = smem + 12288;
+    float* h0arr = smem + 12416 + g*32;
+    float* h1l   = smem + 12480;
+    float* gibH  = smem + 12544;
+    float* harrH = smem + 15616;
+    const float* gsrcL = giL + b*49152 + g*96;
+    const float* gsrcH = giH + b*24576;
+
+    float wI[3][16], wH[3][16];
+    float b0=0.f, b1=0.f, b2=0.f, b3=0.f;
+    #pragma unroll
+    for (int gt = 0; gt < 3; ++gt)
+      #pragma unroll
+      for (int k = 0; k < 16; ++k){ wI[gt][k]=0.f; wH[gt][k]=0.f; }
+    if (wid < 4){
+      if (role == 0){
+        #pragma unroll
+        for (int gt = 0; gt < 3; ++gt){
+          const float* w = whhL + (g*96 + gt*32 + h)*32 + ko;
+          #pragma unroll
+          for (int k = 0; k < 16; ++k){ wI[gt][k] = w[k]; wH[gt][k] = w[k]; }
+        }
+        b0 = bhhL[g*96+h]; b1 = bhhL[g*96+32+h]; b2 = bhhL[g*96+64+h];
+        #pragma unroll
+        for (int c0 = 0; c0 < 2; ++c0)
+          for (int it = 0; it < 12; ++it){
+            int i = it*64 + lane;
+            int toff = i/24, c4 = i - toff*24;
+            gload16(gsrcL + (c0*32 + toff)*192 + c4*4, &smem[g*6144 + c0*3072 + it*256]);
+          }
+        asm volatile("s_waitcnt vmcnt(0)" ::: "memory");
+      } else {
+        #pragma unroll
+        for (int gt = 0; gt < 3; ++gt){
+          const float* wi = wihL + ((2+g)*96 + gt*32 + h)*32 + ko;
+          const float* wh = whhL + ((2+g)*96 + gt*32 + h)*32 + ko;
+          #pragma unroll
+          for (int k = 0; k < 16; ++k){ wI[gt][k] = wi[k]; wH[gt][k] = wh[k]; }
+        }
+        b0 = bihL[(2+g)*96+h]    + bhhL[(2+g)*96+h];
+        b1 = bihL[(2+g)*96+32+h] + bhhL[(2+g)*96+32+h];
+        b2 = bihL[(2+g)*96+64+h];
+        b3 = bhhL[(2+g)*96+64+h];
+      }
+    } else {
+      #pragma unroll
+      for (int gt = 0; gt < 3; ++gt){
+        const float* wp = whhH + (gH*48 + gt*16 + hH)*16 + koH;
+        #pragma unroll
+        for (int k = 0; k < 8; ++k) wI[gt][k] = wp[k];
+      }
+      b0 = bhhH[gH*48+hH]; b1 = bhhH[gH*48+16+hH]; b2 = bhhH[gH*48+32+hH];
+      #pragma unroll
+      for (int c0 = 0; c0 < 2; ++c0)
+        for (int it = 0; it < 6; ++it)
+          gload16(gsrcH + c0*1536 + it*256 + lane*4, &gibH[c0*1536 + it*256]);
+      asm volatile("s_waitcnt vmcnt(0)" ::: "memory");
+    }
     #pragma unroll
     for (int gt = 0; gt < 3; ++gt){
-      const float* wp = whhH + (g*48 + gt*16 + h)*16 + ko;
-      #pragma unroll
-      for (int k = 0; k < 8; ++k) ah[gt][k] = wp[k];
-    }
-    #pragma unroll
-    for (int gt = 0; gt < 3; ++gt){
-      #pragma unroll
-      for (int k = 0; k < 8; ++k) KEEP(ah[gt][k]);
-    }
-    const float bhr = bhhH[g*48+h], bhz = bhhH[g*48+16+h], bhn = bhhH[g*48+32+h];
-    const float* gsrc = giH + b*24576;
-    #pragma unroll
-    for (int c0 = 0; c0 < 2; ++c0)
-      for (int it = 0; it < 6; ++it)
-        gload16(gsrc + c0*1536 + it*256 + lane*4, &gib[c0*1536 + it*256]);
-    asm volatile("s_waitcnt vmcnt(0)" ::: "memory");
-
-    float hv[8];
-    #pragma unroll
-    for (int k = 0; k < 8; ++k) hv[k] = 0.f;
+      #pragma unroll
+      for (int k = 0; k < 16; ++k){ KEEP(wI[gt][k]); KEEP(wH[gt][k]); }
+    }
+    __syncthreads();
+
+    float hv[16];
+    #pragma unroll
+    for (int k = 0; k < 16; ++k) hv[k] = 0.f;
     float hOwn = 0.f;
     float c_r = 0.f, c_z = 0.f, c_n = 0.f, p_r = 0.f, p_z = 0.f, p_n = 0.f;
-
-    for (int t = 0; t < Tn; ++t){
-      if ((t & 15) == 0){
-        if (t){
-          int c = t >> 4;
-          if (c < 15){
-            const float* gs = gsrc + (c+1)*1536;
-            for (int it = 0; it < 6; ++it)
-              gload16(gs + it*256 + lane*4, &gib[((c+1)&1)*1536 + it*256]);
-            asm volatile("s_waitcnt vmcnt(6)" ::: "memory");
-          } else {
-            asm volatile("s_waitcnt vmcnt(0)" ::: "memory");
-          }
-        }
-        const float* gt = &gib[((t>>4)&1)*1536 + (t&15)*96 + g*48];
-        c_r = gt[h]; c_z = gt[16+h]; c_n = gt[32+h];
-      } else { c_r = p_r; c_z = p_z; c_n = p_n; }
-      if ((t+1) & 15){
-        const float* gn = &gib[(((t+1)>>4)&1)*1536 + ((t+1)&15)*96 + g*48];
-        p_r = gn[h]; p_z = gn[16+h]; p_n = gn[32+h];
-      }
-      float pr, pz, pn;
-      DOT8(pr, hv, ah[0]); DOT8(pz, hv, ah[1]); DOT8(pn, hv, ah[2]);
-      pr += __shfl_xor(pr,16); pz += __shfl_xor(pz,16); pn += __shfl_xor(pn,16);
-      float r = fsig(c_r + pr + bhr);
-      float z = fsig(c_z + pz + bhz);
-      float nn = ftanh(c_n + r*(pn + bhn));
-      float hn = nn + z*(hOwn - nn);
-      hOwn = hn;
-      harr[g*16 + h] = hn;
-      *(float4*)&hv[0] = *(const float4*)&harr[g*16 + ko + 0];
-      *(float4*)&hv[4] = *(const float4*)&harr[g*16 + ko + 4];
-      if (qh == 0) dfh[(b*256 + t)*32 + g*16 + h] = hn;
+    const int spos = ((h&1)<<5) + (g<<4) + (h>>1);
+
+    for (int s = 0; s <= Tn; ++s){
+      __syncthreads();
+      if (wid < 4){
+        if (role == 0){
+          if (s < Tn){
+            const int t = s;
+            if ((t & 31) == 0){
+              if (t){
+                int c = t >> 5;
+                if (c < 7){
+                  for (int it = 0; it < 12; ++it){
+                    int i = it*64 + lane;
+                    int toff = i/24, c4 = i - toff*24;
+                    gload16(gsrcL + ((c+1)*32 + toff)*192 + c4*4, &smem[g*6144 + ((c+1)&1)*3072 + it*256]);
+                  }
+                }
+              }
+              const float* gt = &smem[g*6144 + ((t>>5)&1)*3072 + (t&31)*96];
+              c_r = gt[h]; c_z = gt[32+h]; c_n = gt[64+h];
+            } else { c_r = p_r; c_z = p_z; c_n = p_n; }
+            if ((t+1) & 31){
+              const float* gn = &smem[g*6144 + (((t+1)>>5)&1)*3072 + ((t+1)&31)*96];
+              p_r = gn[h]; p_z = gn[32+h]; p_n = gn[64+h];
+            }
+            float pr, pz, pn;
+            DOT16(pr, hv, wI[0]); DOT16(pz, hv, wI[1]); DOT16(pn, hv, wI[2]);
+            pr += __shfl_xor(pr,32); pz += __shfl_xor(pz,32); pn += __shfl_xor(pn,32);
+            float r = fsig(c_r + pr + b0);
+            float z = fsig(c_z + pz + b1);
+            float nn = ftanh(c_n + r*(pn + b2));
+            float hn = nn + z*(hOwn - nn);
+            hOwn = hn;
+            h0arr[h] = hn;
+            if (q == 0) y0buf[(s&1)*64 + spos] = hn;
+            *(float4*)&hv[0]  = *(const float4*)&h0arr[ko+0];
+            *(float4*)&hv[4]  = *(const float4*)&h0arr[ko+4];
+            *(float4*)&hv[8]  = *(const float4*)&h0arr[ko+8];
+            *(float4*)&hv[12] = *(const float4*)&h0arr[ko+12];
+          }
+        } else {
+          if (s >= 1){
+            const int t = s - 1;
+            const float* yb = &y0buf[(t&1)*64];
+            float xv[16];
+            *(float4*)&xv[0]  = *(const float4*)&yb[g*32 + ko + 0];
+            *(float4*)&xv[4]  = *(const float4*)&yb[g*32 + ko + 4];
+            *(float4*)&xv[8]  = *(const float4*)&yb[g*32 + ko + 8];
+            *(float4*)&xv[12] = *(const float4*)&yb[g*32 + ko + 12];
+            float yown = yb[g*32 + h];
+            float ur, uz, ui, vr, vz, vh;
+            DOT16(ur, xv, wI[0]); DOT16(uz, xv, wI[1]); DOT16(ui, xv, wI[2]);
+            DOT16(vr, hv, wH[0]); DOT16(vz, hv, wH[1]); DOT16(vh, hv, wH[2]);
+            float qr = ur + vr, qz = uz + vz;
+            qr += __shfl_xor(qr,32); qz += __shfl_xor(qz,32);
+            ui += __shfl_xor(ui,32); vh += __shfl_xor(vh,32);
+            float r1 = fsig(qr + b0);
+            float z1 = fsig(qz + b1);
+            float n1 = ftanh(ui + b2 + r1*(vh + b3));
+            float hn = n1 + z1*(hOwn - n1);
+            hOwn = hn;
+            h1l[g*32 + h] = hn;
+            *(float4*)&hv[0]  = *(const float4*)&h1l[g*32 + ko+0];
+            *(float4*)&hv[4]  = *(const float4*)&h1l[g*32 + ko+4];
+            *(float4*)&hv[8]  = *(const float4*)&h1l[g*32 + ko+8];
+            *(float4*)&hv[12] = *(const float4*)&h1l[g*32 + ko+12];
+            if (q == 0) acc[(b*256 + t)*64 + g*32 + h] = yown + hn;
+          }
+        }
+      } else {
+        if (s < Tn){
+          const int t = s;
+          if ((t & 15) == 0){
+            if (t){
+              int c = t >> 4;
+              if (c < 15){
+                const float* gs = gsrcH + (c+1)*1536;
+                for (int it = 0; it < 6; ++it)
+                  gload16(gs + it*256 + lane*4, &gibH[((c+1)&1)*1536 + it*256]);
+                asm volatile("s_waitcnt vmcnt(6)" ::: "memory");
+              } else {
+                asm volatile("s_waitcnt vmcnt(0)" ::: "memory");
+              }
+            }
+            const float* gt = &gibH[((t>>4)&1)*1536 + (t&15)*96 + gH*48];
+            c_r = gt[hH]; c_z = gt[16+hH]; c_n = gt[32+hH];
+          } else { c_r = p_r; c_z = p_z; c_n = p_n; }
+          if ((t+1) & 15){
+            const float* gn = &gibH[(((t+1)>>4)&1)*1536 + ((t+1)&15)*96 + gH*48];
+            p_r = gn[hH]; p_z = gn[16+hH]; p_n = gn[32+hH];
+          }
+          float pr, pz, pn;
+          DOT8(pr, hv, wI[0]); DOT8(pz, hv, wI[1]); DOT8(pn, hv, wI[2]);
+          pr += __shfl_xor(pr,16); pz += __shfl_xor(pz,16); pn += __shfl_xor(pn,16);
+          float r = fsig(c_r + pr + b0);
+          float z = fsig(c_z + pz + b1);
+          float nn = ftanh(c_n + r*(pn + b2));
+          float hn = nn + z*(hOwn - nn);
+          hOwn = hn;
+          harrH[gH*16 + hH] = hn;
+          *(float4*)&hv[0] = *(const float4*)&harrH[gH*16 + koH + 0];
+          *(float4*)&hv[4] = *(const float4*)&harrH[gH*16 + koH + 4];
+          if (qH == 0) dfh[(b*256 + t)*32 + gH*16 + hH] = hn;
+        }
+      }
     }
   }
 }
@@ -744,28 +734,24 @@
 
   float* outf = (float*)d_out;
   float* giL  = outf;
-  float* gi0  = outf + 12582912;
+  float* gi0w = outf + 12582912;
   float* giH  = outf + 18874368;
 
-  float* ws    = (float*)d_ws;
-  float* wcT   = ws;
-  float* bc    = ws + 6144;
-  float* wBT   = ws + 6240;
-  float* bB    = ws + 13920;
-  float* wih1T = ws + 14208;
-  float* wB2T  = ws + 17280;
-  float* bB2   = ws + 23424;
-  float* bmA   = ws + 24576;
-  float* acc   = ws + 2121728;
-  float* dfh   = ws + 6316032;
-  float* out   = (float*)d_out;
-
-  k0<<<93, 256, 0, stream>>>(s1w, s1b, wih0, bih0, wih1, glw_ih, glb_ih, ghw_ih, ghb_ih,
-                             wcT, bc, wBT, bB, wih1T, wB2T, bB2);
-  k1<<<2048, 256, 0, stream>>>(mi, wcT, bc, gi0);
-  kS1<<<256, 128, 0, stream>>>(gi0, whh0, bhh0, wih1, whh1, bih1, bhh1, fco, bmA);
-  kP<<<2048, 256, 0, stream>>>(lpi, bmA, filw, plo, fihw, phi, wBT, bB, giL, giH);
-  kR2<<<320, 256, 0, stream>>>(giL, giH, glw_ih, glw_hh, glb_ih, glb_hh,
-                               ghw_hh, ghb_hh, acc, dfh);
+  float* ws  = (float*)d_ws;
+  float* wcT = ws;
+  float* bc  = ws + 6144;
+  float* wBT = ws + 6240;
+  float* bB  = ws + 13920;
+  float* bmA = ws + 14336;
+  float* acc = ws + 2111488;
+  float* dfh = ws + 6305792;
+  float* out = (float*)d_out;
+
+  k0<<<56, 256, 0, stream>>>(s1w, s1b, wih0, bih0, glw_ih, glb_ih, ghw_ih, ghb_ih,
+                             wcT, bc, wBT, bB);
+  kM<<<256, 320, 0, stream>>>(mi, wcT, bc, whh0, bhh0, wih1, whh1, bih1, bhh1, fco,
+                              lpi, filw, plo, fihw, phi, wBT, bB,
+                              glw_ih, glw_hh, glb_ih, glb_hh, ghw_hh, ghb_hh,
+                              gi0w, bmA, giL, giH, acc, dfh);
   k7<<<2048, 256, 0, stream>>>(acc, dfh, bmA, folw, fohw, spec, out);
 }
```

New measurement: 633.1 us. 1.09x slower.
